# Kernel tuning notes

Hardware: AMD Instinct MI355X
Metric: run time of the kernel (lower is better)

## Reference

```python
import jax, jax.numpy as jnp
import numpy as np
from math import factorial

# irreps as (mul, l, parity): hidden = 64x0e + 32x1o + 16x2e (dim 240), edge = 1x0e + 1x1o (dim 4)
HIDDEN = [(64, 0, 1), (32, 1, -1), (16, 2, 1)]
EDGE = [(1, 0, 1), (1, 1, -1)]
N_LAYERS = 6
N_NODES = 10000
N_EDGES = 160000
N_GRAPHS = 64
IN_DIM = 3
LATENT = 128  # config.LATENT_DIM_GNN
W_STD = 0.1   # weight scale keeps 6 residual bilinear layers numerically stable

def _dim(ir):
    return sum(m * (2 * l + 1) for m, l, _ in ir)

def _slices(ir):
    out, o = [], 0
    for m, l, _ in ir:
        d = m * (2 * l + 1)
        out.append(slice(o, o + d))
        o += d
    return out

def _cg(j1, m1, j2, m2, j3, m3):
    # Condon-Shortley Clebsch-Gordan <j1 m1 j2 m2 | j3 m3> (Racah formula)
    if m1 + m2 != m3:
        return 0.0
    f = lambda n: float(factorial(n))
    pre = ((2 * j3 + 1) * f(j3 + j1 - j2) * f(j3 - j1 + j2) * f(j1 + j2 - j3) / f(j1 + j2 + j3 + 1)) ** 0.5
    pre *= (f(j3 + m3) * f(j3 - m3) * f(j1 - m1) * f(j1 + m1) * f(j2 - m2) * f(j2 + m2)) ** 0.5
    s = 0.0
    for k in range(j1 + j2 - j3 + 1):
        a = [k, j1 + j2 - j3 - k, j1 - m1 - k, j2 + m2 - k, j3 - j2 + m1 + k, j3 - j1 - m2 + k]
        if any(t < 0 for t in a):
            continue
        s += (-1) ** k / np.prod([f(t) for t in a])
    return pre * s

def _w3j_complex(l1, l2, l3):
    W = np.zeros((2 * l1 + 1, 2 * l2 + 1, 2 * l3 + 1))
    for m1 in range(-l1, l1 + 1):
        for m2 in range(-l2, l2 + 1):
            m3 = -(m1 + m2)
            if abs(m3) > l3:
                continue
            W[m1 + l1, m2 + l2, m3 + l3] = (-1) ** (l1 - l2 - m3) / np.sqrt(2 * l3 + 1) * _cg(l1, m1, l2, m2, l3, -m3)
    return W

def _A_real(l):
    # real SH in terms of complex SH: Y^r_m = sum_mu A[m, mu] Y_mu
    A = np.zeros((2 * l + 1, 2 * l + 1), dtype=complex)
    A[l, l] = 1.0
    for m in range(1, l + 1):
        A[l + m, l + m] = (-1) ** m / np.sqrt(2)
        A[l + m, l - m] = 1 / np.sqrt(2)
        A[l - m, l + m] = -1j * (-1) ** m / np.sqrt(2)
        A[l - m, l - m] = 1j / np.sqrt(2)
    return A

_W3J_CACHE = {}
def real_w3j(l1, l2, l3):
    key = (l1, l2, l3)
    if key not in _W3J_CACHE:
        T = np.einsum('ad,be,cf,def->abc', _A_real(l1), _A_real(l2), _A_real(l3), _w3j_complex(l1, l2, l3).astype(complex))
        T = np.real(T)  # exactly real when l1+l2+l3 is even (true for all paths here)
        _W3J_CACHE[key] = (T / np.linalg.norm(T)).astype(np.float32)
    return _W3J_CACHE[key]

def _paths(ir1, ir2, irout):
    ps = []
    for i1, (_, l1, p1) in enumerate(ir1):
        for i2, (_, l2, p2) in enumerate(ir2):
            for i3, (_, l3, p3) in enumerate(irout):
                if p3 == p1 * p2 and abs(l1 - l2) <= l3 <= l1 + l2:
                    ps.append((i1, i2, i3))
    return ps

MSG_PATHS = _paths(HIDDEN, EDGE, HIDDEN)
UPD_PATHS = _paths(HIDDEN, HIDDEN, HIDDEN)

def _tp_wsize(ir1, ir2, irout, paths):
    return sum(ir1[a][0] * ir2[b][0] * irout[c][0] for a, b, c in paths)

MSG_WSIZE = _tp_wsize(HIDDEN, EDGE, HIDDEN, MSG_PATHS)
UPD_WSIZE = _tp_wsize(HIDDEN, HIDDEN, HIDDEN, UPD_PATHS)
LIN_WSIZE = sum(m * m for m, _, _ in HIDDEN)

def tensor_product(x1, x2, w_flat, ir1, ir2, irout, paths):
    # FullyConnectedTensorProduct: per-path CG-coupled bilinear op with path normalization
    s1, s2, s3 = _slices(ir1), _slices(ir2), _slices(irout)
    npo = [0] * len(irout)
    for _, _, i3 in paths:
        npo[i3] += 1
    out = jnp.zeros((x1.shape[0], _dim(irout)), dtype=x1.dtype)
    off = 0
    for i1, i2, i3 in paths:
        m1, l1, _ = ir1[i1]; m2, l2, _ = ir2[i2]; m3, l3, _ = irout[i3]
        W = w_flat[off:off + m1 * m2 * m3].reshape(m1, m2, m3)
        off += m1 * m2 * m3
        C = jnp.asarray(real_w3j(l1, l2, l3), dtype=x1.dtype)
        a = x1[:, s1[i1]].reshape(-1, m1, 2 * l1 + 1)
        b = x2[:, s2[i2]].reshape(-1, m2, 2 * l2 + 1)
        alpha = 1.0 / np.sqrt(m1 * m2 * npo[i3])
        y = alpha * jnp.einsum('nui,nvj,uvw,ijk->nwk', a, b, W, C)
        out = out.at[:, s3[i3]].add(y.reshape(-1, m3 * (2 * l3 + 1)))
    return out

def irreps_linear(x, w_flat, ir):
    # e3nn Linear with identical in/out irreps: per-irrep mixing of multiplicities
    sl = _slices(ir)
    parts, off = [], 0
    for i, (m, l, _) in enumerate(ir):
        W = w_flat[off:off + m * m].reshape(m, m)
        off += m * m
        xi = x[:, sl[i]].reshape(-1, m, 2 * l + 1)
        parts.append((jnp.einsum('nui,uv->nvi', xi, W) / np.sqrt(m)).reshape(-1, m * (2 * l + 1)))
    return jnp.concatenate(parts, axis=-1)

def _forward(x, pos, w_init, w_tp_msg, w_lin_msg, w_tp_upd, w_lin_upd, w_final, edge_index, batch):
    row, col = edge_index[0], edge_index[1]
    r_vec = pos[row] - pos[col]                           # (E, 3)
    dist = jnp.linalg.norm(r_vec, axis=-1, keepdims=True)
    nvec = r_vec / jnp.maximum(dist, 1e-8)
    edge_attr = jnp.concatenate([dist, nvec], axis=-1)    # layer consumes [dist, r_vec] = 1x0e + 1x1o
    h = jnp.zeros((x.shape[0], _dim(HIDDEN)), dtype=x.dtype)
    h = h.at[:, :64].set(x @ w_init / np.sqrt(IN_DIM))    # initial Linear hits only 0e channels
    for L in range(N_LAYERS):
        hj = h[col]  # gather neighbor (source) features
        msg = tensor_product(hj, edge_attr, w_tp_msg[L], HIDDEN, EDGE, HIDDEN, MSG_PATHS) \
            + irreps_linear(hj, w_lin_msg[L], HIDDEN)
        agg = jax.ops.segment_sum(msg, row, num_segments=N_NODES)  # scatter-add aggregate
        upd = tensor_product(h, agg, w_tp_upd[L], HIDDEN, HIDDEN, HIDDEN, UPD_PATHS) \
            + irreps_linear(h, w_lin_upd[L], HIDDEN)
        h = h + upd  # residual
    scal = h[:, :64]  # 0e (invariant) channels
    cnt = jax.ops.segment_sum(jnp.ones((x.shape[0],), x.dtype), batch, num_segments=N_GRAPHS)
    pooled = jax.ops.segment_sum(scal, batch, num_segments=N_GRAPHS) / jnp.maximum(cnt, 1.0)[:, None]
    return pooled @ w_final / np.sqrt(64)

def setup_inputs() -> dict:
    key = jax.random.key(0)
    ks = jax.random.split(key, 10)
    return {
        'x': jax.random.normal(ks[0], (N_NODES, IN_DIM), jnp.float32),
        'pos': jax.random.normal(ks[1], (N_NODES, 3), jnp.float32),
        'w_init': jax.random.normal(ks[2], (IN_DIM, 64), jnp.float32),
        'w_tp_msg': jax.random.normal(ks[3], (N_LAYERS, MSG_WSIZE), jnp.float32) * W_STD,
        'w_lin_msg': jax.random.normal(ks[4], (N_LAYERS, LIN_WSIZE), jnp.float32) * W_STD,
        'w_tp_upd': jax.random.normal(ks[5], (N_LAYERS, UPD_WSIZE), jnp.float32) * W_STD,
        'w_lin_upd': jax.random.normal(ks[6], (N_LAYERS, LIN_WSIZE), jnp.float32) * W_STD,
        'w_final': jax.random.normal(ks[7], (64, LATENT), jnp.float32),
        'edge_index': jax.random.randint(ks[8], (2, N_EDGES), 0, N_NODES),
        'batch': jnp.sort(jax.random.randint(ks[9], (N_NODES,), 0, N_GRAPHS)),
    }

def reference(x, pos, w_init, w_tp_msg, w_lin_msg, w_tp_upd, w_lin_upd, w_final, edge_index, batch):
    return _forward(x, pos, w_init, w_tp_msg, w_lin_msg, w_tp_upd, w_lin_upd, w_final, edge_index, batch)
```

## Files before the change

### kernel.cpp

```cpp
#include <hip/hip_runtime.h>
#include <cmath>
#include <cstring>
#include <complex>

#define NN 10000
#define NE 160000
#define HD 240
#define ZD 912
#define NG 64
#define MSG_WS 10496
#define UPD_WS 561152
#define LIN_WS 5376

struct CMsgPre { float a000, a011, a110, a112, a211; float c101[9]; float c202[25]; };
struct CEdge   { float c011[9]; float c110[9]; float c112[45]; float c211[45]; };
struct CUpdS   { float s000; float c011[9]; float c022[25]; float c101[9]; float c202[25]; };
struct CUpdD   { float c110[9]; float c220[25]; };
struct CUpdP   { float c112[45]; float c121[45]; float c211[45]; float c222[125]; };


__global__ __launch_bounds__(256) void k_edge_attr(
    const float* __restrict__ pos, const int* __restrict__ ei, CEdge C,
    float* __restrict__ EA, float* __restrict__ CN) {
  int e = blockIdx.x * 256 + threadIdx.x;
  if (e >= NE) return;
  int r = ei[e], c = ei[NE + e];
  float dx = pos[r*3+0] - pos[c*3+0];
  float dy = pos[r*3+1] - pos[c*3+1];
  float dz = pos[r*3+2] - pos[c*3+2];
  float d = sqrtf(dx*dx + dy*dy + dz*dz);
  float inv = 1.0f / fmaxf(d, 1e-8f);
  float n0 = dx*inv, n1 = dy*inv, n2 = dz*inv;
  EA[e*4+0] = d; EA[e*4+1] = n0; EA[e*4+2] = n1; EA[e*4+3] = n2;
  float* cn = CN + (size_t)e*36;
#pragma unroll
  for (int k = 0; k < 3; k++)
    cn[k] = n0*C.c011[0*3+k] + n1*C.c011[1*3+k] + n2*C.c011[2*3+k];
#pragma unroll
  for (int i = 0; i < 3; i++)
    cn[3+i] = n0*C.c110[i*3+0] + n1*C.c110[i*3+1] + n2*C.c110[i*3+2];
#pragma unroll
  for (int i = 0; i < 3; i++)
#pragma unroll
    for (int k = 0; k < 5; k++)
      cn[6+i*5+k] = n0*C.c112[(i*3+0)*5+k] + n1*C.c112[(i*3+1)*5+k] + n2*C.c112[(i*3+2)*5+k];
#pragma unroll
  for (int i = 0; i < 5; i++)
#pragma unroll
    for (int k = 0; k < 3; k++)
      cn[21+i*3+k] = n0*C.c211[(i*3+0)*3+k] + n1*C.c211[(i*3+1)*3+k] + n2*C.c211[(i*3+2)*3+k];
}

__global__ __launch_bounds__(256) void k_h_init(
    const float* __restrict__ x, const float* __restrict__ wi, float* __restrict__ HT) {
  int n = blockIdx.x * 256 + threadIdx.x;
  int e = blockIdx.y;
  if (n >= NN) return;
  float v = 0.f;
  if (e < 64)
    v = (x[n*3+0]*wi[0*64+e] + x[n*3+1]*wi[64+e] + x[n*3+2]*wi[128+e]) * 0.57735026918962576f;
  HT[e*NN + n] = v;
}

__global__ __launch_bounds__(256) void k_node_pre(
    const float* __restrict__ HT, const float* __restrict__ Wm, const float* __restrict__ Wl,
    CMsgPre C, float* __restrict__ Z) {
  int n = blockIdx.x * 256 + threadIdx.x;
  int widx = blockIdx.y;
  if (n >= NN) return;
  float acc = 0.f;
  if (widx < 64) {
    int w = widx;
    for (int u = 0; u < 64; u++) acc += HT[u*NN+n] * Wm[u*64+w];
    acc *= C.a000;
  } else if (widx < 96) {
    int w = widx - 64;
    for (int u = 0; u < 64; u++) acc += HT[u*NN+n] * Wm[4096 + u*32+w];
    acc *= C.a011;
  } else if (widx < 192) {
    int t = widx - 96, w = t/3, k = t - w*3;
    for (int u = 0; u < 32; u++) {
      float g = HT[(64+u*3+0)*NN+n]*C.c101[0*3+k]
              + HT[(64+u*3+1)*NN+n]*C.c101[1*3+k]
              + HT[(64+u*3+2)*NN+n]*C.c101[2*3+k];
      acc += Wm[6144 + u*32+w] * g;
    }
  } else if (widx < 384) {
    int t = widx - 192, w = t/3, i = t - w*3;
    for (int u = 0; u < 32; u++) acc += HT[(64+u*3+i)*NN+n] * Wm[7168 + u*64+w];
    acc *= C.a110;
  } else if (widx < 432) {
    int t = widx - 384, w = t/3, i = t - w*3;
    for (int u = 0; u < 32; u++) acc += HT[(64+u*3+i)*NN+n] * Wm[9216 + u*16+w];
    acc *= C.a112;
  } else if (widx < 512) {
    int t = widx - 432, w = t/5, k = t - w*5;
    for (int u = 0; u < 16; u++) {
      float g = 0.f;
#pragma unroll
      for (int i = 0; i < 5; i++) g += HT[(160+u*5+i)*NN+n] * C.c202[i*5+k];
      acc += Wm[9728 + u*16+w] * g;
    }
  } else if (widx < 672) {
    int t = widx - 512, w = t/5, i = t - w*5;
    for (int u = 0; u < 16; u++) acc += HT[(160+u*5+i)*NN+n] * Wm[9984 + u*32+w];
    acc *= C.a211;
  } else {
    int e2 = widx - 672;
    if (e2 < 64) {
      for (int u = 0; u < 64; u++) acc += HT[u*NN+n] * Wl[u*64+e2];
      acc *= 0.125f;
    } else if (e2 < 160) {
      int t = e2 - 64, v = t/3, i = t - v*3;
      for (int u = 0; u < 32; u++) acc += HT[(64+u*3+i)*NN+n] * Wl[4096 + u*32+v];
      acc *= 0.17677669529663687f;
    } else {
      int t = e2 - 160, v = t/5, i = t - v*5;
      for (int u = 0; u < 16; u++) acc += HT[(160+u*5+i)*NN+n] * Wl[5120 + u*16+v];
      acc *= 0.25f;
    }
  }
  Z[(size_t)n*ZD + widx] = acc;
}

__global__ __launch_bounds__(256) void k_edge(
    const int* __restrict__ ei, const float* __restrict__ EA, const float* __restrict__ CN,
    const float* __restrict__ Z, float* __restrict__ AGG) {
  __shared__ float zsh[4][ZD];
  int lane = threadIdx.x & 63, wid = threadIdx.x >> 6;
  int wg = blockIdx.x * 4 + wid;
  int stride = gridDim.x * 4;
  int iters = (NE + stride - 1) / stride;
  for (int it = 0; it < iters; ++it) {
    int e = wg + it * stride;
    bool act = e < NE;
    int r = 0;
    float s = 0.f;
    const float* cn = CN;
    if (act) {
      r = ei[e];
      int c = ei[NE + e];
      s = EA[e*4];
      cn = CN + (size_t)e*36;
      const float* zr = Z + (size_t)c*ZD;
      for (int t = lane; t < ZD; t += 64) zsh[wid][t] = zr[t];
    }
    __syncthreads();
    if (act) {
      const float* z = zsh[wid];
#pragma unroll
      for (int j = 0; j < 4; j++) {
        int idx = lane + 64*j;
        if (idx < HD) {
          float y = z[672 + idx];
          if (idx < 64) {
            int w = idx;
            y += s * z[w];
#pragma unroll
            for (int i = 0; i < 3; i++) y += z[192 + w*3 + i] * cn[3+i];
          } else if (idx < 160) {
            int t = idx - 64, w = t/3, k = t - w*3;
            y += cn[k] * z[64 + w] + s * z[96 + t];
#pragma unroll
            for (int i = 0; i < 5; i++) y += z[512 + w*5 + i] * cn[21 + i*3 + k];
          } else {
            int t = idx - 160, w = t/5, k = t - w*5;
            y += s * z[432 + t];
#pragma unroll
            for (int i = 0; i < 3; i++) y += z[384 + w*3 + i] * cn[6 + i*5 + k];
          }
          atomicAdd(&AGG[(size_t)r*HD + idx], y);
        }
      }
    }
    __syncthreads();
  }
}

__global__ __launch_bounds__(256) void k_transpose(
    const float* __restrict__ A_nm, float* __restrict__ A_t) {
  int n = blockIdx.x * 256 + threadIdx.x;
  int e = blockIdx.y;
  if (n >= NN) return;
  A_t[e*NN + n] = A_nm[(size_t)n*HD + e];
}

__global__ __launch_bounds__(128, 2) void k_upd(
    const float* __restrict__ A,
    const float* __restrict__ B,
    const float* __restrict__ W,
    CUpdS CS, CUpdD CD, CUpdP CP,
    float* __restrict__ UPD) {
  __shared__ float4 lds4[1024];
  const int tid = threadIdx.x;
  const int n0 = blockIdx.x * 256 + tid;
  const int n1 = n0 + 128;
  const bool ok0 = n0 < NN, ok1 = n1 < NN;
  const int nc0 = ok0 ? n0 : NN - 1;
  const int nc1 = ok1 ? n1 : NN - 1;
  const int py = blockIdx.y;

#define LDA2(dst, e) { int _e=(e); dst.x = A[_e*NN+nc0]; dst.y = A[_e*NN+nc1]; }
#define LDB2(dst, e) { int _e=(e); dst.x = B[_e*NN+nc0]; dst.y = B[_e*NN+nc1]; }

  if (py < 16) {
    const int w04 = py;
    float2 y[4];
#pragma unroll
    for (int w = 0; w < 4; w++) y[w] = make_float2(0.f, 0.f);

    {
      const float4* W4 = (const float4*)W;
      for (int uc = 0; uc < 4; ++uc) {
        __syncthreads();
        for (int t = tid; t < 1024; t += 128) lds4[t] = W4[(uc*1024 + t)*16 + w04];
        __syncthreads();
        float2 ha[16];
#pragma unroll
        for (int u = 0; u < 16; ++u) {
          LDA2(ha[u], uc*16 + u);
          ha[u].x *= CS.s000; ha[u].y *= CS.s000;
        }
        for (int v = 0; v < 64; ++v) {
          float2 bv; LDB2(bv, v);
#pragma unroll
          for (int u = 0; u < 16; ++u) {
            float4 wl = lds4[u*64 + v];
            float px = ha[u].x * bv.x, qx = ha[u].y * bv.y;
            y[0].x += px*wl.x; y[0].y += qx*wl.x;
            y[1].x += px*wl.y; y[1].y += qx*wl.y;
            y[2].x += px*wl.z; y[2].y += qx*wl.z;
            y[3].x += px*wl.w; y[3].y += qx*wl.w;
          }
        }
      }
    }

    {
      const float4* W4 = (const float4*)(W + 409600);
      __syncthreads();
      for (int t = tid; t < 1024; t += 128) lds4[t] = W4[t*16 + w04];
      __syncthreads();
      for (int uc = 0; uc < 4; ++uc) {
        float2 a[8][3];
#pragma unroll
        for (int u = 0; u < 8; ++u)
#pragma unroll
          for (int i = 0; i < 3; ++i) LDA2(a[u][i], 64 + (uc*8+u)*3 + i);
        for (int v = 0; v < 32; ++v) {
          float2 b[3];
#pragma unroll
          for (int j = 0; j < 3; ++j) LDB2(b[j], 64 + v*3 + j);
          float2 bt[3];
#pragma unroll
          for (int i = 0; i < 3; ++i) {
            bt[i].x = CD.c110[i*3+0]*b[0].x + CD.c110[i*3+1]*b[1].x + CD.c110[i*3+2]*b[2].x;
            bt[i].y = CD.c110[i*3+0]*b[0].y + CD.c110[i*3+1]*b[1].y + CD.c110[i*3+2]*b[2].y;
          }
#pragma unroll
          for (int u = 0; u < 8; ++u) {
            float Dx = a[u][0].x*bt[0].x + a[u][1].x*bt[1].x + a[u][2].x*bt[2].x;
            float Dy = a[u][0].y*bt[0].y + a[u][1].y*bt[1].y + a[u][2].y*bt[2].y;
            float4 wl = lds4[(uc*8+u)*32 + v];
            y[0].x += Dx*wl.x; y[0].y += Dy*wl.x;
            y[1].x += Dx*wl.y; y[1].y += Dy*wl.y;
            y[2].x += Dx*wl.z; y[2].y += Dy*wl.z;
            y[3].x += Dx*wl.w; y[3].y += Dy*wl.w;
          }
        }
      }
    }

    {
      const float4* W4 = (const float4*)(W + 540672);
      __syncthreads();
      for (int t = tid; t < 256; t += 128) lds4[t] = W4[t*16 + w04];
      __syncthreads();
      for (int uc = 0; uc < 4; ++uc) {
        float2 a[4][5];
#pragma unroll
        for (int u = 0; u < 4; ++u)
#pragma unroll
          for (int i = 0; i < 5; ++i) LDA2(a[u][i], 160 + (uc*4+u)*5 + i);
        for (int v = 0; v < 16; ++v) {
          float2 b[5];
#pragma unroll
          for (int j = 0; j < 5; ++j) LDB2(b[j], 160 + v*5 + j);
          float2 bt[5];
#pragma unroll
          for (int i = 0; i < 5; ++i) {
            float tx = 0.f, ty = 0.f;
#pragma unroll
            for (int j = 0; j < 5; ++j) { tx += CD.c220[i*5+j]*b[j].x; ty += CD.c220[i*5+j]*b[j].y; }
            bt[i].x = tx; bt[i].y = ty;
          }
#pragma unroll
          for (int u = 0; u < 4; ++u) {
            float Dx = 0.f, Dy = 0.f;
#pragma unroll
            for (int i = 0; i < 5; ++i) { Dx += a[u][i].x*bt[i].x; Dy += a[u][i].y*bt[i].y; }
            float4 wl = lds4[(uc*4+u)*16 + v];
            y[0].x += Dx*wl.x; y[0].y += Dy*wl.x;
            y[1].x += Dx*wl.y; y[1].y += Dy*wl.y;
            y[2].x += Dx*wl.z; y[2].y += Dy*wl.z;
            y[3].x += Dx*wl.w; y[3].y += Dy*wl.w;
          }
        }
      }
    }

#pragma unroll
    for (int w = 0; w < 4; ++w) {
      if (ok0) UPD[(py*4 + w)*NN + n0] = y[w].x;
      if (ok1) UPD[(py*4 + w)*NN + n1] = y[w].y;
    }

  } else if (py < 24) {
    const int w04 = py - 16;
    float2 y[4][3];
#pragma unroll
    for (int w = 0; w < 4; w++)
#pragma unroll
      for (int k = 0; k < 3; k++) y[w][k] = make_float2(0.f, 0.f);

    {
      const float4* W4 = (const float4*)(W + 262144);
      for (int uc = 0; uc < 2; ++uc) {
        __syncthreads();
        for (int t = tid; t < 1024; t += 128) lds4[t] = W4[(uc*1024 + t)*8 + w04];
        __syncthreads();
        float2 a[32];
#pragma unroll
        for (int u = 0; u < 32; ++u) LDA2(a[u], uc*32 + u);
        for (int v = 0; v < 32; ++v) {
          float2 b[3];
#pragma unroll
          for (int j = 0; j < 3; ++j) LDB2(b[j], 64 + v*3 + j);
          float2 bc[3];
#pragma unroll
          for (int k = 0; k < 3; ++k) {
            bc[k].x = b[0].x*CS.c011[k] + b[1].x*CS.c011[3+k] + b[2].x*CS.c011[6+k];
            bc[k].y = b[0].y*CS.c011[k] + b[1].y*CS.c011[3+k] + b[2].y*CS.c011[6+k];
          }
          float2 g[4];
#pragma unroll
          for (int w = 0; w < 4; w++) g[w] = make_float2(0.f, 0.f);
#pragma unroll
          for (int u = 0; u < 32; ++u) {
            float4 wl = lds4[u*32 + v];
            g[0].x += a[u].x*wl.x; g[0].y += a[u].y*wl.x;
            g[1].x += a[u].x*wl.y; g[1].y += a[u].y*wl.y;
            g[2].x += a[u].x*wl.z; g[2].y += a[u].y*wl.z;
            g[3].x += a[u].x*wl.w; g[3].y += a[u].y*wl.w;
          }
#pragma unroll
          for (int w = 0; w < 4; ++w)
#pragma unroll
            for (int k = 0; k < 3; ++k) {
              y[w][k].x += bc[k].x*g[w].x; y[w][k].y += bc[k].y*g[w].y;
            }
        }
      }
    }

    {
      const float4* W4 = (const float4*)(W + 344064);
      for (int uc = 0; uc < 2; ++uc) {
        __syncthreads();
        for (int t = tid; t < 1024; t += 128) lds4[t] = W4[(uc*1024 + t)*8 + w04];
        __syncthreads();
        for (int vc = 0; vc < 4; ++vc) {
          float2 bv[16];
#pragma unroll
          for (int v2 = 0; v2 < 16; ++v2) LDB2(bv[v2], vc*16 + v2);
          for (int u = 0; u < 16; ++u) {
            float2 aa[3];
#pragma unroll
            for (int i = 0; i < 3; ++i) LDA2(aa[i], 64 + (uc*16+u)*3 + i);
            float2 ac[3];
#pragma unroll
            for (int k = 0; k < 3; ++k) {
              ac[k].x = aa[0].x*CS.c101[k] + aa[1].x*CS.c101[3+k] + aa[2].x*CS.c101[6+k];
              ac[k].y = aa[0].y*CS.c101[k] + aa[1].y*CS.c101[3+k] + aa[2].y*CS.c101[6+k];
            }
            float2 gp[4];
#pragma unroll
            for (int w = 0; w < 4; w++) gp[w] = make_float2(0.f, 0.f);
#pragma unroll
            for (int v2 = 0; v2 < 16; ++v2) {
              float4 wl = lds4[u*64 + vc*16 + v2];
              gp[0].x += bv[v2].x*wl.x; gp[0].y += bv[v2].y*wl.x;
              gp[1].x += bv[v2].x*wl.y; gp[1].y += bv[v2].y*wl.y;
              gp[2].x += bv[v2].x*wl.z; gp[2].y += bv[v2].y*wl.z;
              gp[3].x += bv[v2].x*wl.w; gp[3].y += bv[v2].y*wl.w;
            }
#pragma unroll
            for (int w = 0; w < 4; ++w)
#pragma unroll
              for (int k = 0; k < 3; ++k) {
                y[w][k].x += ac[k].x*gp[w].x; y[w][k].y += ac[k].y*gp[w].y;
              }
          }
        }
      }
    }

    {
      const float4* W4 = (const float4*)(W + 491520);
      __syncthreads();
      for (int t = tid; t < 512; t += 128) lds4[t] = W4[t*8 + w04];
      __syncthreads();
      for (int uc = 0; uc < 4; ++uc) {
        float2 a[8][3];
#pragma unroll
        for (int u = 0; u < 8; ++u)
#pragma unroll
          for (int i = 0; i < 3; ++i) LDA2(a[u][i], 64 + (uc*8+u)*3 + i);
        for (int v = 0; v < 16; ++v) {
          float2 b[5];
#pragma unroll
          for (int j = 0; j < 5; ++j) LDB2(b[j], 160 + v*5 + j);
          float2 bt[3][3];
#pragma unroll
          for (int i = 0; i < 3; ++i)
#pragma unroll
            for (int k = 0; k < 3; ++k) {
              float tx = 0.f, ty = 0.f;
#pragma unroll
              for (int j = 0; j < 5; ++j) { tx += b[j].x*CP.c121[(i*5+j)*3+k]; ty += b[j].y*CP.c121[(i*5+j)*3+k]; }
              bt[i][k].x = tx; bt[i][k].y = ty;
            }
#pragma unroll
          for (int u = 0; u < 8; ++u) {
            float2 P[3];
#pragma unroll
            for (int k = 0; k < 3; ++k) {
              P[k].x = a[u][0].x*bt[0][k].x + a[u][1].x*bt[1][k].x + a[u][2].x*bt[2][k].x;
              P[k].y = a[u][0].y*bt[0][k].y + a[u][1].y*bt[1][k].y + a[u][2].y*bt[2][k].y;
            }
            float4 wl = lds4[(uc*8+u)*16 + v];
#pragma unroll
            for (int k = 0; k < 3; ++k) {
              y[0][k].x += P[k].x*wl.x; y[0][k].y += P[k].y*wl.x;
              y[1][k].x += P[k].x*wl.y; y[1][k].y += P[k].y*wl.y;
              y[2][k].x += P[k].x*wl.z; y[2][k].y += P[k].y*wl.z;
              y[3][k].x += P[k].x*wl.w; y[3][k].y += P[k].y*wl.w;
            }
          }
        }
      }
    }

    {
      const float4* W4 = (const float4*)(W + 524288);
      __syncthreads();
      for (int t = tid; t < 512; t += 128) lds4[t] = W4[t*8 + w04];
      __syncthreads();
      for (int uc = 0; uc < 2; ++uc) {
        float2 a[8][5];
#pragma unroll
        for (int u = 0; u < 8; ++u)
#pragma unroll
          for (int i = 0; i < 5; ++i) LDA2(a[u][i], 160 + (uc*8+u)*5 + i);
        for (int v = 0; v < 32; ++v) {
          float2 b[3];
#pragma unroll
          for (int j = 0; j < 3; ++j) LDB2(b[j], 64 + v*3 + j);
          float2 bt[5][3];
#pragma unroll
          for (int i = 0; i < 5; ++i)
#pragma unroll
            for (int k = 0; k < 3; ++k) {
              bt[i][k].x = b[0].x*CP.c211[(i*3+0)*3+k] + b[1].x*CP.c211[(i*3+1)*3+k] + b[2].x*CP.c211[(i*3+2)*3+k];
              bt[i][k].y = b[0].y*CP.c211[(i*3+0)*3+k] + b[1].y*CP.c211[(i*3+1)*3+k] + b[2].y*CP.c211[(i*3+2)*3+k];
            }
#pragma unroll
          for (int u = 0; u < 8; ++u) {
            float2 P[3];
#pragma unroll
            for (int k = 0; k < 3; ++k) {
              float tx = 0.f, ty = 0.f;
#pragma unroll
              for (int i = 0; i < 5; ++i) { tx += a[u][i].x*bt[i][k].x; ty += a[u][i].y*bt[i][k].y; }
              P[k].x = tx; P[k].y = ty;
            }
            float4 wl = lds4[(uc*8+u)*32 + v];
#pragma unroll
            for (int k = 0; k < 3; ++k) {
              y[0][k].x += P[k].x*wl.x; y[0][k].y += P[k].y*wl.x;
              y[1][k].x += P[k].x*wl.y; y[1][k].y += P[k].y*wl.y;
              y[2][k].x += P[k].x*wl.z; y[2][k].y += P[k].y*wl.z;
              y[3][k].x += P[k].x*wl.w; y[3][k].y += P[k].y*wl.w;
            }
          }
        }
      }
    }

#pragma unroll
    for (int w = 0; w < 4; ++w)
#pragma unroll
      for (int k = 0; k < 3; ++k) {
        int e = 64 + (w04*4 + w)*3 + k;
        if (ok0) UPD[e*NN + n0] = y[w][k].x;
        if (ok1) UPD[e*NN + n1] = y[w][k].y;
      }

  } else {
    const int w04 = py - 24;
    float2 y[4][5];
#pragma unroll
    for (int w = 0; w < 4; w++)
#pragma unroll
      for (int k = 0; k < 5; k++) y[w][k] = make_float2(0.f, 0.f);

    {
      const float4* W4 = (const float4*)(W + 327680);
      __syncthreads();
      for (int t = tid; t < 1024; t += 128) lds4[t] = W4[t*4 + w04];
      __syncthreads();
      for (int uc = 0; uc < 4; ++uc) {
        float2 a[16];
#pragma unroll
        for (int u = 0; u < 16; ++u) LDA2(a[u], uc*16 + u);
        for (int v = 0; v < 16; ++v) {
          float2 b[5];
#pragma unroll
          for (int j = 0; j < 5; ++j) LDB2(b[j], 160 + v*5 + j);
          float2 bc[5];
#pragma unroll
          for (int k = 0; k < 5; ++k) {
            float tx = 0.f, ty = 0.f;
#pragma unroll
            for (int j = 0; j < 5; ++j) { tx += b[j].x*CS.c022[j*5+k]; ty += b[j].y*CS.c022[j*5+k]; }
            bc[k].x = tx; bc[k].y = ty;
          }
          float2 g[4];
#pragma unroll
          for (int w = 0; w < 4; w++) g[w] = make_float2(0.f, 0.f);
#pragma unroll
          for (int u = 0; u < 16; ++u) {
            float4 wl = lds4[(uc*16+u)*16 + v];
            g[0].x += a[u].x*wl.x; g[0].y += a[u].y*wl.x;
            g[1].x += a[u].x*wl.y; g[1].y += a[u].y*wl.y;
            g[2].x += a[u].x*wl.z; g[2].y += a[u].y*wl.z;
            g[3].x += a[u].x*wl.w; g[3].y += a[u].y*wl.w;
          }
#pragma unroll
          for (int w = 0; w < 4; ++w)
#pragma unroll
            for (int k = 0; k < 5; ++k) {
              y[w][k].x += bc[k].x*g[w].x; y[w][k].y += bc[k].y*g[w].y;
            }
        }
      }
    }

    {
      const float4* W4 = (const float4*)(W + 507904);
      __syncthreads();
      for (int t = tid; t < 1024; t += 128) lds4[t] = W4[t*4 + w04];
      __syncthreads();
      for (int vc = 0; vc < 4; ++vc) {
        float2 bv[16];
#pragma unroll
        for (int v2 = 0; v2 < 16; ++v2) LDB2(bv[v2], vc*16 + v2);
        for (int u = 0; u < 16; ++u) {
          float2 aa[5];
#pragma unroll
          for (int i = 0; i < 5; ++i) LDA2(aa[i], 160 + u*5 + i);
          float2 ac[5];
#pragma unroll
          for (int k = 0; k < 5; ++k) {
            float tx = 0.f, ty = 0.f;
#pragma unroll
            for (int i = 0; i < 5; ++i) { tx += aa[i].x*CS.c202[i*5+k]; ty += aa[i].y*CS.c202[i*5+k]; }
            ac[k].x = tx; ac[k].y = ty;
          }
          float2 gp[4];
#pragma unroll
          for (int w = 0; w < 4; w++) gp[w] = make_float2(0.f, 0.f);
#pragma unroll
          for (int v2 = 0; v2 < 16; ++v2) {
            float4 wl = lds4[u*64 + vc*16 + v2];
            gp[0].x += bv[v2].x*wl.x; gp[0].y += bv[v2].y*wl.x;
            gp[1].x += bv[v2].x*wl.y; gp[1].y += bv[v2].y*wl.y;
            gp[2].x += bv[v2].x*wl.z; gp[2].y += bv[v2].y*wl.z;
            gp[3].x += bv[v2].x*wl.w; gp[3].y += bv[v2].y*wl.w;
          }
#pragma unroll
          for (int w = 0; w < 4; ++w)
#pragma unroll
            for (int k = 0; k < 5; ++k) {
              y[w][k].x += ac[k].x*gp[w].x; y[w][k].y += ac[k].y*gp[w].y;
            }
        }
      }
    }

    {
      const float4* W4 = (const float4*)(W + 475136);
      __syncthreads();
      for (int t = tid; t < 1024; t += 128) lds4[t] = W4[t*4 + w04];
      __syncthreads();
      for (int uc = 0; uc < 4; ++uc) {
        float2 a[8][3];
#pragma unroll
        for (int u = 0; u < 8; ++u)
#pragma unroll
          for (int i = 0; i < 3; ++i) LDA2(a[u][i], 64 + (uc*8+u)*3 + i);
        for (int v = 0; v < 32; ++v) {
          float2 b[3];
#pragma unroll
          for (int j = 0; j < 3; ++j) LDB2(b[j], 64 + v*3 + j);
          float2 bt[3][5];
#pragma unroll
          for (int i = 0; i < 3; ++i)
#pragma unroll
            for (int k = 0; k < 5; ++k) {
              bt[i][k].x = b[0].x*CP.c112[(i*3+0)*5+k] + b[1].x*CP.c112[(i*3+1)*5+k] + b[2].x*CP.c112[(i*3+2)*5+k];
              bt[i][k].y = b[0].y*CP.c112[(i*3+0)*5+k] + b[1].y*CP.c112[(i*3+1)*5+k] + b[2].y*CP.c112[(i*3+2)*5+k];
            }
#pragma unroll
          for (int u = 0; u < 8; ++u) {
            float2 P[5];
#pragma unroll
            for (int k = 0; k < 5; ++k) {
              P[k].x = a[u][0].x*bt[0][k].x + a[u][1].x*bt[1][k].x + a[u][2].x*bt[2][k].x;
              P[k].y = a[u][0].y*bt[0][k].y + a[u][1].y*bt[1][k].y + a[u][2].y*bt[2][k].y;
            }
            float4 wl = lds4[(uc*8+u)*32 + v];
#pragma unroll
            for (int k = 0; k < 5; ++k) {
              y[0][k].x += P[k].x*wl.x; y[0][k].y += P[k].y*wl.x;
              y[1][k].x += P[k].x*wl.y; y[1][k].y += P[k].y*wl.y;
              y[2][k].x += P[k].x*wl.z; y[2][k].y += P[k].y*wl.z;
              y[3][k].x += P[k].x*wl.w; y[3][k].y += P[k].y*wl.w;
            }
          }
        }
      }
    }

    {
      const float4* W4 = (const float4*)(W + 557056);
      __syncthreads();
      for (int t = tid; t < 256; t += 128) lds4[t] = W4[t*4 + w04];
      __syncthreads();
      for (int v = 0; v < 16; ++v) {
        float2 b[5];
#pragma unroll
        for (int j = 0; j < 5; ++j) LDB2(b[j], 160 + v*5 + j);
        float2 bt[5][5];
#pragma unroll
        for (int i = 0; i < 5; ++i)
#pragma unroll
          for (int k = 0; k < 5; ++k) {
            float tx = 0.f, ty = 0.f;
#pragma unroll
            for (int j = 0; j < 5; ++j) { tx += b[j].x*CP.c222[(i*5+j)*5+k]; ty += b[j].y*CP.c222[(i*5+j)*5+k]; }
            bt[i][k].x = tx; bt[i][k].y = ty;
          }
        for (int u = 0; u < 16; ++u) {
          float2 aa[5];
#pragma unroll
          for (int i = 0; i < 5; ++i) LDA2(aa[i], 160 + u*5 + i);
          float2 P[5];
#pragma unroll
          for (int k = 0; k < 5; ++k) {
            float tx = 0.f, ty = 0.f;
#pragma unroll
            for (int i = 0; i < 5; ++i) { tx += aa[i].x*bt[i][k].x; ty += aa[i].y*bt[i][k].y; }
            P[k].x = tx; P[k].y = ty;
          }
          float4 wl = lds4[u*16 + v];
#pragma unroll
          for (int k = 0; k < 5; ++k) {
            y[0][k].x += P[k].x*wl.x; y[0][k].y += P[k].y*wl.x;
            y[1][k].x += P[k].x*wl.y; y[1][k].y += P[k].y*wl.y;
            y[2][k].x += P[k].x*wl.z; y[2][k].y += P[k].y*wl.z;
            y[3][k].x += P[k].x*wl.w; y[3][k].y += P[k].y*wl.w;
          }
        }
      }
    }

#pragma unroll
    for (int w = 0; w < 4; ++w)
#pragma unroll
      for (int k = 0; k < 5; ++k) {
        int e = 160 + (w04*4 + w)*5 + k;
        if (ok0) UPD[e*NN + n0] = y[w][k].x;
        if (ok1) UPD[e*NN + n1] = y[w][k].y;
      }
  }
#undef LDA2
#undef LDB2
}

__global__ __launch_bounds__(256) void k_apply(
    const float* __restrict__ Hsrc, const float* __restrict__ UPD,
    const float* __restrict__ Wl, float* __restrict__ Hdst) {
  int n = blockIdx.x * 256 + threadIdx.x;
  int e = blockIdx.y;
  if (n >= NN) return;
  float lin = 0.f;
  if (e < 64) {
    for (int u = 0; u < 64; u++) lin += Hsrc[u*NN+n] * Wl[u*64+e];
    lin *= 0.125f;
  } else if (e < 160) {
    int t = e - 64, v = t/3, i = t - v*3;
    for (int u = 0; u < 32; u++) lin += Hsrc[(64+u*3+i)*NN+n] * Wl[4096 + u*32+v];
    lin *= 0.17677669529663687f;
  } else {
    int t = e - 160, v = t/5, i = t - v*5;
    for (int u = 0; u < 16; u++) lin += Hsrc[(160+u*5+i)*NN+n] * Wl[5120 + u*16+v];
    lin *= 0.25f;
  }
  Hdst[e*NN + n] = Hsrc[e*NN + n] + UPD[e*NN + n] + lin;
}

__global__ __launch_bounds__(256) void k_cnt(const int* __restrict__ batch, float* __restrict__ CNT) {
  int n = blockIdx.x * 256 + threadIdx.x;
  if (n >= NN) return;
  atomicAdd(&CNT[batch[n]], 1.0f);
}

__global__ __launch_bounds__(256) void k_pool(
    const float* __restrict__ HT, const int* __restrict__ batch, float* __restrict__ POOL) {
  int n = blockIdx.x * 256 + threadIdx.x;
  int w = blockIdx.y;
  if (n >= NN) return;
  atomicAdd(&POOL[batch[n]*64 + w], HT[w*NN + n]);
}

__global__ __launch_bounds__(256) void k_out(
    const float* __restrict__ POOL, const float* __restrict__ CNT,
    const float* __restrict__ wf, float* __restrict__ out) {
  int tid = blockIdx.x * 256 + threadIdx.x;
  if (tid >= NG * 128) return;
  int g = tid >> 7, d = tid & 127;
  float inv = 1.0f / fmaxf(CNT[g], 1.0f);
  float acc = 0.f;
  for (int w = 0; w < 64; w++) acc += POOL[g*64 + w] * wf[w*128 + d];
  out[tid] = acc * inv * 0.125f;
}

typedef std::complex<double> cd;
static double hfact(int nn) { double f = 1; for (int i = 2; i <= nn; i++) f *= i; return f; }
static double hcg(int j1,int m1,int j2,int m2,int j3,int m3) {
  if (m1 + m2 != m3) return 0.0;
  double pre = sqrt((2*j3+1) * hfact(j3+j1-j2) * hfact(j3-j1+j2) * hfact(j1+j2-j3) / hfact(j1+j2+j3+1));
  pre *= sqrt(hfact(j3+m3)*hfact(j3-m3)*hfact(j1-m1)*hfact(j1+m1)*hfact(j2-m2)*hfact(j2+m2));
  double s = 0;
  for (int k = 0; k <= j1+j2-j3; k++) {
    int a1=j1+j2-j3-k, a2=j1-m1-k, a3=j2+m2-k, a4=j3-j2+m1+k, a5=j3-j1-m2+k;
    if (a1<0||a2<0||a3<0||a4<0||a5<0) continue;
    s += ((k&1)?-1.0:1.0) / (hfact(k)*hfact(a1)*hfact(a2)*hfact(a3)*hfact(a4)*hfact(a5));
  }
  return pre * s;
}
static void hA(int l, cd A[5][5]) {
  for (int r = 0; r < 5; r++) for (int c = 0; c < 5; c++) A[r][c] = cd(0,0);
  A[l][l] = cd(1,0);
  for (int m = 1; m <= l; m++) {
    double sg = (m & 1) ? -1.0 : 1.0;
    A[l+m][l+m] = cd(sg/sqrt(2.0), 0);
    A[l+m][l-m] = cd(1.0/sqrt(2.0), 0);
    A[l-m][l+m] = cd(0, -sg/sqrt(2.0));
    A[l-m][l-m] = cd(0, 1.0/sqrt(2.0));
  }
}
static void hw3j(int l1, int l2, int l3, double* out) {
  int n1 = 2*l1+1, n2 = 2*l2+1, n3 = 2*l3+1;
  double Wc[5][5][5]; memset(Wc, 0, sizeof Wc);
  for (int m1 = -l1; m1 <= l1; m1++) for (int m2 = -l2; m2 <= l2; m2++) {
    int m3 = -(m1+m2);
    if (m3 < -l3 || m3 > l3) continue;
    int ex = l1 - l2 - m3;
    double sg = (ex % 2 == 0) ? 1.0 : -1.0;
    Wc[m1+l1][m2+l2][m3+l3] = sg / sqrt((double)(2*l3+1)) * hcg(l1,m1,l2,m2,l3,-m3);
  }
  cd A1[5][5], A2[5][5], A3[5][5];
  hA(l1,A1); hA(l2,A2); hA(l3,A3);
  double nrm = 0;
  for (int a = 0; a < n1; a++) for (int b = 0; b < n2; b++) for (int c = 0; c < n3; c++) {
    cd acc(0,0);
    for (int d = 0; d < n1; d++) for (int e = 0; e < n2; e++) for (int f = 0; f < n3; f++) {
      double w = Wc[d][e][f];
      if (w == 0.0) continue;
      acc += A1[a][d] * A2[b][e] * A3[c][f] * w;
    }
    out[(a*n2+b)*n3+c] = acc.real();
    nrm += acc.real() * acc.real();
  }
  nrm = sqrt(nrm);
  for (int i = 0; i < n1*n2*n3; i++) out[i] /= nrm;
}

extern "C" void kernel_launch(void* const* d_in, const int* in_sizes, int n_in,
                              void* d_out, int out_size, void* d_ws, size_t ws_size,
                              hipStream_t stream) {
  const float* x        = (const float*)d_in[0];
  const float* pos      = (const float*)d_in[1];
  const float* w_init   = (const float*)d_in[2];
  const float* w_tp_msg = (const float*)d_in[3];
  const float* w_lin_msg= (const float*)d_in[4];
  const float* w_tp_upd = (const float*)d_in[5];
  const float* w_lin_upd= (const float*)d_in[6];
  const float* w_final  = (const float*)d_in[7];
  const int*   ei       = (const int*)d_in[8];
  const int*   batch    = (const int*)d_in[9];
  float* out = (float*)d_out;
  float* ws  = (float*)d_ws;

  float* EA     = ws;
  float* CN     = EA + 640000;
  float* HTA    = CN + 5760000;
  float* HTB    = HTA + 2400000;
  float* Z      = HTB + 2400000;
  float* AGG_NM = Z + 9120000;
  float* UPD_T  = AGG_NM + 2400000;
  float* AGG_T  = UPD_T + 2400000;
  float* POOL   = AGG_T + 2400000;
  float* CNT    = POOL + 4096;

  double C000d[1], C011d[9], C101d[9], C110d[9], C112d[45], C022d[25],
         C202d[25], C121d[45], C211d[45], C220d[25], C222d[125];
  hw3j(0,0,0,C000d); hw3j(0,1,1,C011d); hw3j(1,0,1,C101d); hw3j(1,1,0,C110d);
  hw3j(1,1,2,C112d); hw3j(0,2,2,C022d); hw3j(2,0,2,C202d); hw3j(1,2,1,C121d);
  hw3j(2,1,1,C211d); hw3j(2,2,0,C220d); hw3j(2,2,2,C222d);

  CMsgPre cmsg;
  cmsg.a000 = (float)(C000d[0] / sqrt(128.0));
  cmsg.a011 = (float)(1.0 / sqrt(192.0));
  cmsg.a110 = (float)(1.0 / sqrt(64.0));
  cmsg.a112 = (float)(1.0 / sqrt(64.0));
  cmsg.a211 = (float)(1.0 / sqrt(48.0));
  for (int i = 0; i < 9;  i++) cmsg.c101[i] = (float)(C101d[i] / sqrt(96.0));
  for (int i = 0; i < 25; i++) cmsg.c202[i] = (float)(C202d[i] / sqrt(32.0));

  CEdge ce;
  for (int i = 0; i < 9;  i++) ce.c011[i] = (float)C011d[i];
  for (int i = 0; i < 9;  i++) ce.c110[i] = (float)C110d[i];
  for (int i = 0; i < 45; i++) ce.c112[i] = (float)C112d[i];
  for (int i = 0; i < 45; i++) ce.c211[i] = (float)C211d[i];

  CUpdS cus;
  cus.s000 = (float)(C000d[0] / sqrt(64.0*64.0*3.0));
  for (int i = 0; i < 9;  i++) cus.c011[i] = (float)(C011d[i] / sqrt(64.0*32.0*4.0));
  for (int i = 0; i < 25; i++) cus.c022[i] = (float)(C022d[i] / sqrt(64.0*16.0*4.0));
  for (int i = 0; i < 9;  i++) cus.c101[i] = (float)(C101d[i] / sqrt(32.0*64.0*4.0));
  for (int i = 0; i < 25; i++) cus.c202[i] = (float)(C202d[i] / sqrt(16.0*64.0*4.0));

  CUpdD cud;
  for (int i = 0; i < 9;  i++) cud.c110[i] = (float)(C110d[i] / sqrt(32.0*32.0*3.0));
  for (int i = 0; i < 25; i++) cud.c220[i] = (float)(C220d[i] / sqrt(16.0*16.0*3.0));

  CUpdP cup;
  for (int i = 0; i < 45;  i++) cup.c112[i] = (float)(C112d[i] / sqrt(32.0*32.0*4.0));
  for (int i = 0; i < 45;  i++) cup.c121[i] = (float)(C121d[i] / sqrt(32.0*16.0*4.0));
  for (int i = 0; i < 45;  i++) cup.c211[i] = (float)(C211d[i] / sqrt(16.0*32.0*4.0));
  for (int i = 0; i < 125; i++) cup.c222[i] = (float)(C222d[i] / sqrt(16.0*16.0*4.0));

  k_edge_attr<<<(NE+255)/256, 256, 0, stream>>>(pos, ei, ce, EA, CN);
  k_h_init<<<dim3(40, HD), 256, 0, stream>>>(x, w_init, HTA);

  float* cur = HTA;
  float* nxt = HTB;
  for (int L = 0; L < 6; L++) {
    hipMemsetAsync(AGG_NM, 0, (size_t)2400000 * sizeof(float), stream);
    k_node_pre<<<dim3(40, ZD), 256, 0, stream>>>(cur, w_tp_msg + (size_t)L*MSG_WS,
                                                 w_lin_msg + (size_t)L*LIN_WS, cmsg, Z);
    k_edge<<<1280, 256, 0, stream>>>(ei, EA, CN, Z, AGG_NM);
    k_transpose<<<dim3(40, HD), 256, 0, stream>>>(AGG_NM, AGG_T);
    const float* Wu = w_tp_upd + (size_t)L*UPD_WS;
    k_upd<<<dim3(40, 28), 128, 0, stream>>>(cur, AGG_T, Wu, cus, cud, cup, UPD_T);
    k_apply<<<dim3(40, HD), 256, 0, stream>>>(cur, UPD_T, w_lin_upd + (size_t)L*LIN_WS, nxt);
    float* tmp = cur; cur = nxt; nxt = tmp;
  }

  hipMemsetAsync(POOL, 0, (size_t)(4096 + 64) * sizeof(float), stream);
  k_cnt<<<(NN+255)/256, 256, 0, stream>>>(batch, CNT);
  k_pool<<<dim3(40, 64), 256, 0, stream>>>(cur, batch, POOL);
  k_out<<<32, 256, 0, stream>>>(POOL, CNT, w_final, out);
}
```

Measured before the change: 5.464 ms.

## Split update tensor-product kernel into per-path pieces reduced with atomics

Each update block used to run several tensor-product paths in sequence. Now every path is its own block piece, and each piece is split four ways along one input-channel axis. Partial sums are added into the output with atomicAdd, so the grid grows from 28 to 384 pieces in y, and the launch bounds ask for 4 blocks per CU for more occupancy. The memset is widened to 4.8M floats, apparently so the atomic destination UPD_T (assumed to sit right after AGG_NM) gets zeroed. The cost is many more global atomics and repeated loads of A and B across pieces.

```diff
diff --git a/kernel.cpp b/kernel.cpp
--- a/kernel.cpp
+++ b/kernel.cpp
@@ -185,7 +185,7 @@
   A_t[e*NN + n] = A_nm[(size_t)n*HD + e];
 }
 
-__global__ __launch_bounds__(128, 2) void k_upd(
+__global__ __launch_bounds__(128, 4) void k_upd(
     const float* __restrict__ A,
     const float* __restrict__ B,
     const float* __restrict__ W,
@@ -198,482 +198,462 @@
   const bool ok0 = n0 < NN, ok1 = n1 < NN;
   const int nc0 = ok0 ? n0 : NN - 1;
   const int nc1 = ok1 ? n1 : NN - 1;
-  const int py = blockIdx.y;
+  const int piece = blockIdx.y;
+  const int rc = piece & 3;
+  const int pt = piece >> 2;
+  const float4* W4 = (const float4*)W;
 
 #define LDA2(dst, e) { int _e=(e); dst.x = A[_e*NN+nc0]; dst.y = A[_e*NN+nc1]; }
 #define LDB2(dst, e) { int _e=(e); dst.x = B[_e*NN+nc0]; dst.y = B[_e*NN+nc1]; }
-
-  if (py < 16) {
-    const int w04 = py;
+#define ATOM2(e, val) { int _e=(e); if (ok0) atomicAdd(&UPD[_e*NN+n0], val.x); if (ok1) atomicAdd(&UPD[_e*NN+n1], val.y); }
+
+  if (pt < 16) {
+    const int w04 = pt, u0 = rc << 4;
+    for (int t = tid; t < 1024; t += 128)
+      lds4[t] = W4[((u0 + (t >> 6)) * 64 + (t & 63)) * 16 + w04];
+    __syncthreads();
+    float2 ha[16];
+#pragma unroll
+    for (int u = 0; u < 16; ++u) {
+      LDA2(ha[u], u0 + u);
+      ha[u].x *= CS.s000; ha[u].y *= CS.s000;
+    }
     float2 y[4];
 #pragma unroll
     for (int w = 0; w < 4; w++) y[w] = make_float2(0.f, 0.f);
-
-    {
-      const float4* W4 = (const float4*)W;
-      for (int uc = 0; uc < 4; ++uc) {
-        __syncthreads();
-        for (int t = tid; t < 1024; t += 128) lds4[t] = W4[(uc*1024 + t)*16 + w04];
-        __syncthreads();
-        float2 ha[16];
+    for (int v = 0; v < 64; ++v) {
+      float2 bv; LDB2(bv, v);
+#pragma unroll
+      for (int u = 0; u < 16; ++u) {
+        float4 wl = lds4[u*64 + v];
+        float px = ha[u].x * bv.x, qx = ha[u].y * bv.y;
+        y[0].x += px*wl.x; y[0].y += qx*wl.x;
+        y[1].x += px*wl.y; y[1].y += qx*wl.y;
+        y[2].x += px*wl.z; y[2].y += qx*wl.z;
+        y[3].x += px*wl.w; y[3].y += qx*wl.w;
+      }
+    }
+#pragma unroll
+    for (int w = 0; w < 4; ++w) ATOM2(w04*4 + w, y[w]);
+
+  } else if (pt < 32) {
+    const int w04 = pt - 16, v0 = rc << 3;
+    for (int t = tid; t < 256; t += 128)
+      lds4[t] = W4[102400 + ((t >> 3) * 32 + v0 + (t & 7)) * 16 + w04];
+    __syncthreads();
+    float2 y[4];
+#pragma unroll
+    for (int w = 0; w < 4; w++) y[w] = make_float2(0.f, 0.f);
+    for (int uc = 0; uc < 4; ++uc) {
+      float2 a[8][3];
+#pragma unroll
+      for (int u = 0; u < 8; ++u)
+#pragma unroll
+        for (int i = 0; i < 3; ++i) LDA2(a[u][i], 64 + (uc*8+u)*3 + i);
+      for (int vl = 0; vl < 8; ++vl) {
+        float2 b[3];
+#pragma unroll
+        for (int j = 0; j < 3; ++j) LDB2(b[j], 64 + (v0+vl)*3 + j);
+        float2 bt[3];
+#pragma unroll
+        for (int i = 0; i < 3; ++i) {
+          bt[i].x = CD.c110[i*3+0]*b[0].x + CD.c110[i*3+1]*b[1].x + CD.c110[i*3+2]*b[2].x;
+          bt[i].y = CD.c110[i*3+0]*b[0].y + CD.c110[i*3+1]*b[1].y + CD.c110[i*3+2]*b[2].y;
+        }
+#pragma unroll
+        for (int u = 0; u < 8; ++u) {
+          float Dx = a[u][0].x*bt[0].x + a[u][1].x*bt[1].x + a[u][2].x*bt[2].x;
+          float Dy = a[u][0].y*bt[0].y + a[u][1].y*bt[1].y + a[u][2].y*bt[2].y;
+          float4 wl = lds4[(uc*8+u)*8 + vl];
+          y[0].x += Dx*wl.x; y[0].y += Dy*wl.x;
+          y[1].x += Dx*wl.y; y[1].y += Dy*wl.y;
+          y[2].x += Dx*wl.z; y[2].y += Dy*wl.z;
+          y[3].x += Dx*wl.w; y[3].y += Dy*wl.w;
+        }
+      }
+    }
+#pragma unroll
+    for (int w = 0; w < 4; ++w) ATOM2(w04*4 + w, y[w]);
+
+  } else if (pt < 48) {
+    const int w04 = pt - 32, v0 = rc << 2;
+    for (int t = tid; t < 64; t += 128)
+      lds4[t] = W4[135168 + ((t >> 2) * 16 + v0 + (t & 3)) * 16 + w04];
+    __syncthreads();
+    float2 y[4];
+#pragma unroll
+    for (int w = 0; w < 4; w++) y[w] = make_float2(0.f, 0.f);
+    for (int uc = 0; uc < 4; ++uc) {
+      float2 a[4][5];
+#pragma unroll
+      for (int u = 0; u < 4; ++u)
+#pragma unroll
+        for (int i = 0; i < 5; ++i) LDA2(a[u][i], 160 + (uc*4+u)*5 + i);
+      for (int vl = 0; vl < 4; ++vl) {
+        float2 b[5];
+#pragma unroll
+        for (int j = 0; j < 5; ++j) LDB2(b[j], 160 + (v0+vl)*5 + j);
+        float2 bt[5];
+#pragma unroll
+        for (int i = 0; i < 5; ++i) {
+          float tx = 0.f, ty = 0.f;
+#pragma unroll
+          for (int j = 0; j < 5; ++j) { tx += CD.c220[i*5+j]*b[j].x; ty += CD.c220[i*5+j]*b[j].y; }
+          bt[i].x = tx; bt[i].y = ty;
+        }
+#pragma unroll
+        for (int u = 0; u < 4; ++u) {
+          float Dx = 0.f, Dy = 0.f;
+#pragma unroll
+          for (int i = 0; i < 5; ++i) { Dx += a[u][i].x*bt[i].x; Dy += a[u][i].y*bt[i].y; }
+          float4 wl = lds4[(uc*4+u)*4 + vl];
+          y[0].x += Dx*wl.x; y[0].y += Dy*wl.x;
+          y[1].x += Dx*wl.y; y[1].y += Dy*wl.y;
+          y[2].x += Dx*wl.z; y[2].y += Dy*wl.z;
+          y[3].x += Dx*wl.w; y[3].y += Dy*wl.w;
+        }
+      }
+    }
+#pragma unroll
+    for (int w = 0; w < 4; ++w) ATOM2(w04*4 + w, y[w]);
+
+  } else if (pt < 56) {
+    const int w04 = pt - 48, v0 = rc << 3;
+    for (int t = tid; t < 512; t += 128)
+      lds4[t] = W4[65536 + ((t >> 3) * 32 + v0 + (t & 7)) * 8 + w04];
+    __syncthreads();
+    float2 y[4][3];
+#pragma unroll
+    for (int w = 0; w < 4; w++)
+#pragma unroll
+      for (int k = 0; k < 3; k++) y[w][k] = make_float2(0.f, 0.f);
+    for (int uc = 0; uc < 4; ++uc) {
+      float2 a[16];
+#pragma unroll
+      for (int u = 0; u < 16; ++u) LDA2(a[u], uc*16 + u);
+      for (int vl = 0; vl < 8; ++vl) {
+        float2 b[3];
+#pragma unroll
+        for (int j = 0; j < 3; ++j) LDB2(b[j], 64 + (v0+vl)*3 + j);
+        float2 bc[3];
+#pragma unroll
+        for (int k = 0; k < 3; ++k) {
+          bc[k].x = b[0].x*CS.c011[k] + b[1].x*CS.c011[3+k] + b[2].x*CS.c011[6+k];
+          bc[k].y = b[0].y*CS.c011[k] + b[1].y*CS.c011[3+k] + b[2].y*CS.c011[6+k];
+        }
+        float2 g[4];
+#pragma unroll
+        for (int w = 0; w < 4; w++) g[w] = make_float2(0.f, 0.f);
 #pragma unroll
         for (int u = 0; u < 16; ++u) {
-          LDA2(ha[u], uc*16 + u);
-          ha[u].x *= CS.s000; ha[u].y *= CS.s000;
-        }
-        for (int v = 0; v < 64; ++v) {
-          float2 bv; LDB2(bv, v);
-#pragma unroll
-          for (int u = 0; u < 16; ++u) {
-            float4 wl = lds4[u*64 + v];
-            float px = ha[u].x * bv.x, qx = ha[u].y * bv.y;
-            y[0].x += px*wl.x; y[0].y += qx*wl.x;
-            y[1].x += px*wl.y; y[1].y += qx*wl.y;
-            y[2].x += px*wl.z; y[2].y += qx*wl.z;
-            y[3].x += px*wl.w; y[3].y += qx*wl.w;
-          }
-        }
-      }
-    }
-
-    {
-      const float4* W4 = (const float4*)(W + 409600);
-      __syncthreads();
-      for (int t = tid; t < 1024; t += 128) lds4[t] = W4[t*16 + w04];
-      __syncthreads();
-      for (int uc = 0; uc < 4; ++uc) {
-        float2 a[8][3];
-#pragma unroll
-        for (int u = 0; u < 8; ++u)
-#pragma unroll
-          for (int i = 0; i < 3; ++i) LDA2(a[u][i], 64 + (uc*8+u)*3 + i);
-        for (int v = 0; v < 32; ++v) {
-          float2 b[3];
-#pragma unroll
-          for (int j = 0; j < 3; ++j) LDB2(b[j], 64 + v*3 + j);
-          float2 bt[3];
-#pragma unroll
-          for (int i = 0; i < 3; ++i) {
-            bt[i].x = CD.c110[i*3+0]*b[0].x + CD.c110[i*3+1]*b[1].x + CD.c110[i*3+2]*b[2].x;
-            bt[i].y = CD.c110[i*3+0]*b[0].y + CD.c110[i*3+1]*b[1].y + CD.c110[i*3+2]*b[2].y;
-          }
-#pragma unroll
-          for (int u = 0; u < 8; ++u) {
-            float Dx = a[u][0].x*bt[0].x + a[u][1].x*bt[1].x + a[u][2].x*bt[2].x;
-            float Dy = a[u][0].y*bt[0].y + a[u][1].y*bt[1].y + a[u][2].y*bt[2].y;
-            float4 wl = lds4[(uc*8+u)*32 + v];
-            y[0].x += Dx*wl.x; y[0].y += Dy*wl.x;
-            y[1].x += Dx*wl.y; y[1].y += Dy*wl.y;
-            y[2].x += Dx*wl.z; y[2].y += Dy*wl.z;
-            y[3].x += Dx*wl.w; y[3].y += Dy*wl.w;
-          }
-        }
-      }
-    }
-
-    {
-      const float4* W4 = (const float4*)(W + 540672);
-      __syncthreads();
-      for (int t = tid; t < 256; t += 128) lds4[t] = W4[t*16 + w04];
-      __syncthreads();
-      for (int uc = 0; uc < 4; ++uc) {
-        float2 a[4][5];
-#pragma unroll
-        for (int u = 0; u < 4; ++u)
-#pragma unroll
-          for (int i = 0; i < 5; ++i) LDA2(a[u][i], 160 + (uc*4+u)*5 + i);
-        for (int v = 0; v < 16; ++v) {
-          float2 b[5];
-#pragma unroll
-          for (int j = 0; j < 5; ++j) LDB2(b[j], 160 + v*5 + j);
-          float2 bt[5];
-#pragma unroll
-          for (int i = 0; i < 5; ++i) {
+          float4 wl = lds4[(uc*16+u)*8 + vl];
+          g[0].x += a[u].x*wl.x; g[0].y += a[u].y*wl.x;
+          g[1].x += a[u].x*wl.y; g[1].y += a[u].y*wl.y;
+          g[2].x += a[u].x*wl.z; g[2].y += a[u].y*wl.z;
+          g[3].x += a[u].x*wl.w; g[3].y += a[u].y*wl.w;
+        }
+#pragma unroll
+        for (int w = 0; w < 4; ++w)
+#pragma unroll
+          for (int k = 0; k < 3; ++k) {
+            y[w][k].x += bc[k].x*g[w].x; y[w][k].y += bc[k].y*g[w].y;
+          }
+      }
+    }
+#pragma unroll
+    for (int w = 0; w < 4; ++w)
+#pragma unroll
+      for (int k = 0; k < 3; ++k) ATOM2(64 + (w04*4 + w)*3 + k, y[w][k]);
+
+  } else if (pt < 64) {
+    const int w04 = pt - 56, v0 = rc << 4;
+    for (int t = tid; t < 512; t += 128)
+      lds4[t] = W4[86016 + ((t >> 4) * 64 + v0 + (t & 15)) * 8 + w04];
+    __syncthreads();
+    float2 y[4][3];
+#pragma unroll
+    for (int w = 0; w < 4; w++)
+#pragma unroll
+      for (int k = 0; k < 3; k++) y[w][k] = make_float2(0.f, 0.f);
+    float2 bv[16];
+#pragma unroll
+    for (int v2 = 0; v2 < 16; ++v2) LDB2(bv[v2], v0 + v2);
+    for (int u = 0; u < 32; ++u) {
+      float2 aa[3];
+#pragma unroll
+      for (int i = 0; i < 3; ++i) LDA2(aa[i], 64 + u*3 + i);
+      float2 ac[3];
+#pragma unroll
+      for (int k = 0; k < 3; ++k) {
+        ac[k].x = aa[0].x*CS.c101[k] + aa[1].x*CS.c101[3+k] + aa[2].x*CS.c101[6+k];
+        ac[k].y = aa[0].y*CS.c101[k] + aa[1].y*CS.c101[3+k] + aa[2].y*CS.c101[6+k];
+      }
+      float2 gp[4];
+#pragma unroll
+      for (int w = 0; w < 4; w++) gp[w] = make_float2(0.f, 0.f);
+#pragma unroll
+      for (int v2 = 0; v2 < 16; ++v2) {
+        float4 wl = lds4[u*16 + v2];
+        gp[0].x += bv[v2].x*wl.x; gp[0].y += bv[v2].y*wl.x;
+        gp[1].x += bv[v2].x*wl.y; gp[1].y += bv[v2].y*wl.y;
+        gp[2].x += bv[v2].x*wl.z; gp[2].y += bv[v2].y*wl.z;
+        gp[3].x += bv[v2].x*wl.w; gp[3].y += bv[v2].y*wl.w;
+      }
+#pragma unroll
+      for (int w = 0; w < 4; ++w)
+#pragma unroll
+        for (int k = 0; k < 3; ++k) {
+          y[w][k].x += ac[k].x*gp[w].x; y[w][k].y += ac[k].y*gp[w].y;
+        }
+    }
+#pragma unroll
+    for (int w = 0; w < 4; ++w)
+#pragma unroll
+      for (int k = 0; k < 3; ++k) ATOM2(64 + (w04*4 + w)*3 + k, y[w][k]);
+
+  } else if (pt < 72) {
+    const int w04 = pt - 64, v0 = rc << 2;
+    for (int t = tid; t < 128; t += 128)
+      lds4[t] = W4[122880 + ((t >> 2) * 16 + v0 + (t & 3)) * 8 + w04];
+    __syncthreads();
+    float2 y[4][3];
+#pragma unroll
+    for (int w = 0; w < 4; w++)
+#pragma unroll
+      for (int k = 0; k < 3; k++) y[w][k] = make_float2(0.f, 0.f);
+    for (int uc = 0; uc < 4; ++uc) {
+      float2 a[8][3];
+#pragma unroll
+      for (int u = 0; u < 8; ++u)
+#pragma unroll
+        for (int i = 0; i < 3; ++i) LDA2(a[u][i], 64 + (uc*8+u)*3 + i);
+      for (int vl = 0; vl < 4; ++vl) {
+        float2 b[5];
+#pragma unroll
+        for (int j = 0; j < 5; ++j) LDB2(b[j], 160 + (v0+vl)*5 + j);
+        float2 bt[3][3];
+#pragma unroll
+        for (int i = 0; i < 3; ++i)
+#pragma unroll
+          for (int k = 0; k < 3; ++k) {
             float tx = 0.f, ty = 0.f;
 #pragma unroll
-            for (int j = 0; j < 5; ++j) { tx += CD.c220[i*5+j]*b[j].x; ty += CD.c220[i*5+j]*b[j].y; }
-            bt[i].x = tx; bt[i].y = ty;
-          }
-#pragma unroll
-          for (int u = 0; u < 4; ++u) {
-            float Dx = 0.f, Dy = 0.f;
-#pragma unroll
-            for (int i = 0; i < 5; ++i) { Dx += a[u][i].x*bt[i].x; Dy += a[u][i].y*bt[i].y; }
-            float4 wl = lds4[(uc*4+u)*16 + v];
-            y[0].x += Dx*wl.x; y[0].y += Dy*wl.x;
-            y[1].x += Dx*wl.y; y[1].y += Dy*wl.y;
-            y[2].x += Dx*wl.z; y[2].y += Dy*wl.z;
-            y[3].x += Dx*wl.w; y[3].y += Dy*wl.w;
-          }
-        }
-      }
-    }
-
-#pragma unroll
-    for (int w = 0; w < 4; ++w) {
-      if (ok0) UPD[(py*4 + w)*NN + n0] = y[w].x;
-      if (ok1) UPD[(py*4 + w)*NN + n1] = y[w].y;
-    }
-
-  } else if (py < 24) {
-    const int w04 = py - 16;
+            for (int j = 0; j < 5; ++j) { tx += b[j].x*CP.c121[(i*5+j)*3+k]; ty += b[j].y*CP.c121[(i*5+j)*3+k]; }
+            bt[i][k].x = tx; bt[i][k].y = ty;
+          }
+#pragma unroll
+        for (int u = 0; u < 8; ++u) {
+          float2 P[3];
+#pragma unroll
+          for (int k = 0; k < 3; ++k) {
+            P[k].x = a[u][0].x*bt[0][k].x + a[u][1].x*bt[1][k].x + a[u][2].x*bt[2][k].x;
+            P[k].y = a[u][0].y*bt[0][k].y + a[u][1].y*bt[1][k].y + a[u][2].y*bt[2][k].y;
+          }
+          float4 wl = lds4[(uc*8+u)*4 + vl];
+#pragma unroll
+          for (int k = 0; k < 3; ++k) {
+            y[0][k].x += P[k].x*wl.x; y[0][k].y += P[k].y*wl.x;
+            y[1][k].x += P[k].x*wl.y; y[1][k].y += P[k].y*wl.y;
+            y[2][k].x += P[k].x*wl.z; y[2][k].y += P[k].y*wl.z;
+            y[3][k].x += P[k].x*wl.w; y[3][k].y += P[k].y*wl.w;
+          }
+        }
+      }
+    }
+#pragma unroll
+    for (int w = 0; w < 4; ++w)
+#pragma unroll
+      for (int k = 0; k < 3; ++k) ATOM2(64 + (w04*4 + w)*3 + k, y[w][k]);
+
+  } else if (pt < 80) {
+    const int w04 = pt - 72, v0 = rc << 3;
+    for (int t = tid; t < 128; t += 128)
+      lds4[t] = W4[131072 + ((t >> 3) * 32 + v0 + (t & 7)) * 8 + w04];
+    __syncthreads();
     float2 y[4][3];
 #pragma unroll
     for (int w = 0; w < 4; w++)
 #pragma unroll
       for (int k = 0; k < 3; k++) y[w][k] = make_float2(0.f, 0.f);
-
-    {
-      const float4* W4 = (const float4*)(W + 262144);
-      for (int uc = 0; uc < 2; ++uc) {
-        __syncthreads();
-        for (int t = tid; t < 1024; t += 128) lds4[t] = W4[(uc*1024 + t)*8 + w04];
-        __syncthreads();
-        float2 a[32];
-#pragma unroll
-        for (int u = 0; u < 32; ++u) LDA2(a[u], uc*32 + u);
-        for (int v = 0; v < 32; ++v) {
-          float2 b[3];
-#pragma unroll
-          for (int j = 0; j < 3; ++j) LDB2(b[j], 64 + v*3 + j);
-          float2 bc[3];
+    for (int uc = 0; uc < 2; ++uc) {
+      float2 a[8][5];
+#pragma unroll
+      for (int u = 0; u < 8; ++u)
+#pragma unroll
+        for (int i = 0; i < 5; ++i) LDA2(a[u][i], 160 + (uc*8+u)*5 + i);
+      for (int vl = 0; vl < 8; ++vl) {
+        float2 b[3];
+#pragma unroll
+        for (int j = 0; j < 3; ++j) LDB2(b[j], 64 + (v0+vl)*3 + j);
+        float2 bt[5][3];
+#pragma unroll
+        for (int i = 0; i < 5; ++i)
 #pragma unroll
           for (int k = 0; k < 3; ++k) {
-            bc[k].x = b[0].x*CS.c011[k] + b[1].x*CS.c011[3+k] + b[2].x*CS.c011[6+k];
-            bc[k].y = b[0].y*CS.c011[k] + b[1].y*CS.c011[3+k] + b[2].y*CS.c011[6+k];
-          }
-          float2 g[4];
-#pragma unroll
-          for (int w = 0; w < 4; w++) g[w] = make_float2(0.f, 0.f);
-#pragma unroll
-          for (int u = 0; u < 32; ++u) {
-            float4 wl = lds4[u*32 + v];
-            g[0].x += a[u].x*wl.x; g[0].y += a[u].y*wl.x;
-            g[1].x += a[u].x*wl.y; g[1].y += a[u].y*wl.y;
-            g[2].x += a[u].x*wl.z; g[2].y += a[u].y*wl.z;
-            g[3].x += a[u].x*wl.w; g[3].y += a[u].y*wl.w;
-          }
-#pragma unroll
-          for (int w = 0; w < 4; ++w)
-#pragma unroll
-            for (int k = 0; k < 3; ++k) {
-              y[w][k].x += bc[k].x*g[w].x; y[w][k].y += bc[k].y*g[w].y;
-            }
-        }
-      }
-    }
-
-    {
-      const float4* W4 = (const float4*)(W + 344064);
-      for (int uc = 0; uc < 2; ++uc) {
-        __syncthreads();
-        for (int t = tid; t < 1024; t += 128) lds4[t] = W4[(uc*1024 + t)*8 + w04];
-        __syncthreads();
-        for (int vc = 0; vc < 4; ++vc) {
-          float2 bv[16];
-#pragma unroll
-          for (int v2 = 0; v2 < 16; ++v2) LDB2(bv[v2], vc*16 + v2);
-          for (int u = 0; u < 16; ++u) {
-            float2 aa[3];
-#pragma unroll
-            for (int i = 0; i < 3; ++i) LDA2(aa[i], 64 + (uc*16+u)*3 + i);
-            float2 ac[3];
-#pragma unroll
-            for (int k = 0; k < 3; ++k) {
-              ac[k].x = aa[0].x*CS.c101[k] + aa[1].x*CS.c101[3+k] + aa[2].x*CS.c101[6+k];
-              ac[k].y = aa[0].y*CS.c101[k] + aa[1].y*CS.c101[3+k] + aa[2].y*CS.c101[6+k];
-            }
-            float2 gp[4];
-#pragma unroll
-            for (int w = 0; w < 4; w++) gp[w] = make_float2(0.f, 0.f);
-#pragma unroll
-            for (int v2 = 0; v2 < 16; ++v2) {
-              float4 wl = lds4[u*64 + vc*16 + v2];
-              gp[0].x += bv[v2].x*wl.x; gp[0].y += bv[v2].y*wl.x;
-              gp[1].x += bv[v2].x*wl.y; gp[1].y += bv[v2].y*wl.y;
-              gp[2].x += bv[v2].x*wl.z; gp[2].y += bv[v2].y*wl.z;
-              gp[3].x += bv[v2].x*wl.w; gp[3].y += bv[v2].y*wl.w;
-            }
-#pragma unroll
-            for (int w = 0; w < 4; ++w)
-#pragma unroll
-              for (int k = 0; k < 3; ++k) {
-                y[w][k].x += ac[k].x*gp[w].x; y[w][k].y += ac[k].y*gp[w].y;
-              }
-          }
-        }
-      }
-    }
-
-    {
-      const float4* W4 = (const float4*)(W + 491520);
-      __syncthreads();
-      for (int t = tid; t < 512; t += 128) lds4[t] = W4[t*8 + w04];
-      __syncthreads();
-      for (int uc = 0; uc < 4; ++uc) {
-        float2 a[8][3];
-#pragma unroll
-        for (int u = 0; u < 8; ++u)
-#pragma unroll
-          for (int i = 0; i < 3; ++i) LDA2(a[u][i], 64 + (uc*8+u)*3 + i);
-        for (int v = 0; v < 16; ++v) {
-          float2 b[5];
-#pragma unroll
-          for (int j = 0; j < 5; ++j) LDB2(b[j], 160 + v*5 + j);
-          float2 bt[3][3];
-#pragma unroll
-          for (int i = 0; i < 3; ++i)
-#pragma unroll
-            for (int k = 0; k < 3; ++k) {
-              float tx = 0.f, ty = 0.f;
-#pragma unroll
-              for (int j = 0; j < 5; ++j) { tx += b[j].x*CP.c121[(i*5+j)*3+k]; ty += b[j].y*CP.c121[(i*5+j)*3+k]; }
-              bt[i][k].x = tx; bt[i][k].y = ty;
-            }
-#pragma unroll
-          for (int u = 0; u < 8; ++u) {
-            float2 P[3];
-#pragma unroll
-            for (int k = 0; k < 3; ++k) {
-              P[k].x = a[u][0].x*bt[0][k].x + a[u][1].x*bt[1][k].x + a[u][2].x*bt[2][k].x;
-              P[k].y = a[u][0].y*bt[0][k].y + a[u][1].y*bt[1][k].y + a[u][2].y*bt[2][k].y;
-            }
-            float4 wl = lds4[(uc*8+u)*16 + v];
-#pragma unroll
-            for (int k = 0; k < 3; ++k) {
-              y[0][k].x += P[k].x*wl.x; y[0][k].y += P[k].y*wl.x;
-              y[1][k].x += P[k].x*wl.y; y[1][k].y += P[k].y*wl.y;
-              y[2][k].x += P[k].x*wl.z; y[2][k].y += P[k].y*wl.z;
-              y[3][k].x += P[k].x*wl.w; y[3][k].y += P[k].y*wl.w;
-            }
-          }
-        }
-      }
-    }
-
-    {
-      const float4* W4 = (const float4*)(W + 524288);
-      __syncthreads();
-      for (int t = tid; t < 512; t += 128) lds4[t] = W4[t*8 + w04];
-      __syncthreads();
-      for (int uc = 0; uc < 2; ++uc) {
-        float2 a[8][5];
-#pragma unroll
-        for (int u = 0; u < 8; ++u)
-#pragma unroll
-          for (int i = 0; i < 5; ++i) LDA2(a[u][i], 160 + (uc*8+u)*5 + i);
-        for (int v = 0; v < 32; ++v) {
-          float2 b[3];
-#pragma unroll
-          for (int j = 0; j < 3; ++j) LDB2(b[j], 64 + v*3 + j);
-          float2 bt[5][3];
-#pragma unroll
-          for (int i = 0; i < 5; ++i)
-#pragma unroll
-            for (int k = 0; k < 3; ++k) {
-              bt[i][k].x = b[0].x*CP.c211[(i*3+0)*3+k] + b[1].x*CP.c211[(i*3+1)*3+k] + b[2].x*CP.c211[(i*3+2)*3+k];
-              bt[i][k].y = b[0].y*CP.c211[(i*3+0)*3+k] + b[1].y*CP.c211[(i*3+1)*3+k] + b[2].y*CP.c211[(i*3+2)*3+k];
-            }
-#pragma unroll
-          for (int u = 0; u < 8; ++u) {
-            float2 P[3];
-#pragma unroll
-            for (int k = 0; k < 3; ++k) {
-              float tx = 0.f, ty = 0.f;
-#pragma unroll
-              for (int i = 0; i < 5; ++i) { tx += a[u][i].x*bt[i][k].x; ty += a[u][i].y*bt[i][k].y; }
-              P[k].x = tx; P[k].y = ty;
-            }
-            float4 wl = lds4[(uc*8+u)*32 + v];
-#pragma unroll
-            for (int k = 0; k < 3; ++k) {
-              y[0][k].x += P[k].x*wl.x; y[0][k].y += P[k].y*wl.x;
-              y[1][k].x += P[k].x*wl.y; y[1][k].y += P[k].y*wl.y;
-              y[2][k].x += P[k].x*wl.z; y[2][k].y += P[k].y*wl.z;
-              y[3][k].x += P[k].x*wl.w; y[3][k].y += P[k].y*wl.w;
-            }
-          }
-        }
-      }
-    }
-
+            bt[i][k].x = b[0].x*CP.c211[(i*3+0)*3+k] + b[1].x*CP.c211[(i*3+1)*3+k] + b[2].x*CP.c211[(i*3+2)*3+k];
+            bt[i][k].y = b[0].y*CP.c211[(i*3+0)*3+k] + b[1].y*CP.c211[(i*3+1)*3+k] + b[2].y*CP.c211[(i*3+2)*3+k];
+          }
+#pragma unroll
+        for (int u = 0; u < 8; ++u) {
+          float2 P[3];
+#pragma unroll
+          for (int k = 0; k < 3; ++k) {
+            float tx = 0.f, ty = 0.f;
+#pragma unroll
+            for (int i = 0; i < 5; ++i) { tx += a[u][i].x*bt[i][k].x; ty += a[u][i].y*bt[i][k].y; }
+            P[k].x = tx; P[k].y = ty;
+          }
+          float4 wl = lds4[(uc*8+u)*8 + vl];
+#pragma unroll
+          for (int k = 0; k < 3; ++k) {
+            y[0][k].x += P[k].x*wl.x; y[0][k].y += P[k].y*wl.x;
+            y[1][k].x += P[k].x*wl.y; y[1][k].y += P[k].y*wl.y;
+            y[2][k].x += P[k].x*wl.z; y[2][k].y += P[k].y*wl.z;
+            y[3][k].x += P[k].x*wl.w; y[3][k].y += P[k].y*wl.w;
+          }
+        }
+      }
+    }
 #pragma unroll
     for (int w = 0; w < 4; ++w)
 #pragma unroll
-      for (int k = 0; k < 3; ++k) {
-        int e = 64 + (w04*4 + w)*3 + k;
-        if (ok0) UPD[e*NN + n0] = y[w][k].x;
-        if (ok1) UPD[e*NN + n1] = y[w][k].y;
-      }
-
-  } else {
-    const int w04 = py - 24;
+      for (int k = 0; k < 3; ++k) ATOM2(64 + (w04*4 + w)*3 + k, y[w][k]);
+
+  } else if (pt < 84) {
+    const int w04 = pt - 80, v0 = rc << 2;
+    for (int t = tid; t < 256; t += 128)
+      lds4[t] = W4[81920 + ((t >> 2) * 16 + v0 + (t & 3)) * 4 + w04];
+    __syncthreads();
     float2 y[4][5];
 #pragma unroll
     for (int w = 0; w < 4; w++)
 #pragma unroll
       for (int k = 0; k < 5; k++) y[w][k] = make_float2(0.f, 0.f);
-
-    {
-      const float4* W4 = (const float4*)(W + 327680);
-      __syncthreads();
-      for (int t = tid; t < 1024; t += 128) lds4[t] = W4[t*4 + w04];
-      __syncthreads();
-      for (int uc = 0; uc < 4; ++uc) {
-        float2 a[16];
-#pragma unroll
-        for (int u = 0; u < 16; ++u) LDA2(a[u], uc*16 + u);
-        for (int v = 0; v < 16; ++v) {
-          float2 b[5];
-#pragma unroll
-          for (int j = 0; j < 5; ++j) LDB2(b[j], 160 + v*5 + j);
-          float2 bc[5];
+    for (int uc = 0; uc < 4; ++uc) {
+      float2 a[16];
+#pragma unroll
+      for (int u = 0; u < 16; ++u) LDA2(a[u], uc*16 + u);
+      for (int vl = 0; vl < 4; ++vl) {
+        float2 b[5];
+#pragma unroll
+        for (int j = 0; j < 5; ++j) LDB2(b[j], 160 + (v0+vl)*5 + j);
+        float2 bc[5];
+#pragma unroll
+        for (int k = 0; k < 5; ++k) {
+          float tx = 0.f, ty = 0.f;
+#pragma unroll
+          for (int j = 0; j < 5; ++j) { tx += b[j].x*CS.c022[j*5+k]; ty += b[j].y*CS.c022[j*5+k]; }
+          bc[k].x = tx; bc[k].y = ty;
+        }
+        float2 g[4];
+#pragma unroll
+        for (int w = 0; w < 4; w++) g[w] = make_float2(0.f, 0.f);
+#pragma unroll
+        for (int u = 0; u < 16; ++u) {
+          float4 wl = lds4[(uc*16+u)*4 + vl];
+          g[0].x += a[u].x*wl.x; g[0].y += a[u].y*wl.x;
+          g[1].x += a[u].x*wl.y; g[1].y += a[u].y*wl.y;
+          g[2].x += a[u].x*wl.z; g[2].y += a[u].y*wl.z;
+          g[3].x += a[u].x*wl.w; g[3].y += a[u].y*wl.w;
+        }
+#pragma unroll
+        for (int w = 0; w < 4; ++w)
 #pragma unroll
           for (int k = 0; k < 5; ++k) {
-            float tx = 0.f, ty = 0.f;
-#pragma unroll
-            for (int j = 0; j < 5; ++j) { tx += b[j].x*CS.c022[j*5+k]; ty += b[j].y*CS.c022[j*5+k]; }
-            bc[k].x = tx; bc[k].y = ty;
-          }
-          float2 g[4];
-#pragma unroll
-          for (int w = 0; w < 4; w++) g[w] = make_float2(0.f, 0.f);
-#pragma unroll
-          for (int u = 0; u < 16; ++u) {
-            float4 wl = lds4[(uc*16+u)*16 + v];
-            g[0].x += a[u].x*wl.x; g[0].y += a[u].y*wl.x;
-            g[1].x += a[u].x*wl.y; g[1].y += a[u].y*wl.y;
-            g[2].x += a[u].x*wl.z; g[2].y += a[u].y*wl.z;
-            g[3].x += a[u].x*wl.w; g[3].y += a[u].y*wl.w;
-          }
-#pragma unroll
-          for (int w = 0; w < 4; ++w)
-#pragma unroll
-            for (int k = 0; k < 5; ++k) {
-              y[w][k].x += bc[k].x*g[w].x; y[w][k].y += bc[k].y*g[w].y;
-            }
-        }
-      }
-    }
-
-    {
-      const float4* W4 = (const float4*)(W + 507904);
-      __syncthreads();
-      for (int t = tid; t < 1024; t += 128) lds4[t] = W4[t*4 + w04];
-      __syncthreads();
-      for (int vc = 0; vc < 4; ++vc) {
-        float2 bv[16];
-#pragma unroll
-        for (int v2 = 0; v2 < 16; ++v2) LDB2(bv[v2], vc*16 + v2);
-        for (int u = 0; u < 16; ++u) {
-          float2 aa[5];
-#pragma unroll
-          for (int i = 0; i < 5; ++i) LDA2(aa[i], 160 + u*5 + i);
-          float2 ac[5];
+            y[w][k].x += bc[k].x*g[w].x; y[w][k].y += bc[k].y*g[w].y;
+          }
+      }
+    }
+#pragma unroll
+    for (int w = 0; w < 4; ++w)
+#pragma unroll
+      for (int k = 0; k < 5; ++k) ATOM2(160 + (w04*4 + w)*5 + k, y[w][k]);
+
+  } else if (pt < 88) {
+    const int w04 = pt - 84, v0 = rc << 4;
+    for (int t = tid; t < 256; t += 128)
+      lds4[t] = W4[126976 + ((t >> 4) * 64 + v0 + (t & 15)) * 4 + w04];
+    __syncthreads();
+    float2 y[4][5];
+#pragma unroll
+    for (int w = 0; w < 4; w++)
+#pragma unroll
+      for (int k = 0; k < 5; k++) y[w][k] = make_float2(0.f, 0.f);
+    float2 bv[16];
+#pragma unroll
+    for (int v2 = 0; v2 < 16; ++v2) LDB2(bv[v2], v0 + v2);
+    for (int u = 0; u < 16; ++u) {
+      float2 aa[5];
+#pragma unroll
+      for (int i = 0; i < 5; ++i) LDA2(aa[i], 160 + u*5 + i);
+      float2 ac[5];
+#pragma unroll
+      for (int k = 0; k < 5; ++k) {
+        float tx = 0.f, ty = 0.f;
+#pragma unroll
+        for (int i = 0; i < 5; ++i) { tx += aa[i].x*CS.c202[i*5+k]; ty += aa[i].y*CS.c202[i*5+k]; }
+        ac[k].x = tx; ac[k].y = ty;
+      }
+      float2 gp[4];
+#pragma unroll
+      for (int w = 0; w < 4; w++) gp[w] = make_float2(0.f, 0.f);
+#pragma unroll
+      for (int v2 = 0; v2 < 16; ++v2) {
+        float4 wl = lds4[u*16 + v2];
+        gp[0].x += bv[v2].x*wl.x; gp[0].y += bv[v2].y*wl.x;
+        gp[1].x += bv[v2].x*wl.y; gp[1].y += bv[v2].y*wl.y;
+        gp[2].x += bv[v2].x*wl.z; gp[2].y += bv[v2].y*wl.z;
+        gp[3].x += bv[v2].x*wl.w; gp[3].y += bv[v2].y*wl.w;
+      }
+#pragma unroll
+      for (int w = 0; w < 4; ++w)
+#pragma unroll
+        for (int k = 0; k < 5; ++k) {
+          y[w][k].x += ac[k].x*gp[w].x; y[w][k].y += ac[k].y*gp[w].y;
+        }
+    }
+#pragma unroll
+    for (int w = 0; w < 4; ++w)
+#pragma unroll
+      for (int k = 0; k < 5; ++k) ATOM2(160 + (w04*4 + w)*5 + k, y[w][k]);
+
+  } else if (pt < 92) {
+    const int w04 = pt - 88, v0 = rc << 3;
+    for (int t = tid; t < 256; t += 128)
+      lds4[t] = W4[118784 + ((t >> 3) * 32 + v0 + (t & 7)) * 4 + w04];
+    __syncthreads();
+    float2 y[4][5];
+#pragma unroll
+    for (int w = 0; w < 4; w++)
+#pragma unroll
+      for (int k = 0; k < 5; k++) y[w][k] = make_float2(0.f, 0.f);
+    for (int uc = 0; uc < 4; ++uc) {
+      float2 a[8][3];
+#pragma unroll
+      for (int u = 0; u < 8; ++u)
+#pragma unroll
+        for (int i = 0; i < 3; ++i) LDA2(a[u][i], 64 + (uc*8+u)*3 + i);
+      for (int vl = 0; vl < 8; ++vl) {
+        float2 b[3];
+#pragma unroll
+        for (int j = 0; j < 3; ++j) LDB2(b[j], 64 + (v0+vl)*3 + j);
+        float2 bt[3][5];
+#pragma unroll
+        for (int i = 0; i < 3; ++i)
 #pragma unroll
           for (int k = 0; k < 5; ++k) {
-            float tx = 0.f, ty = 0.f;
-#pragma unroll
-            for (int i = 0; i < 5; ++i) { tx += aa[i].x*CS.c202[i*5+k]; ty += aa[i].y*CS.c202[i*5+k]; }
-            ac[k].x = tx; ac[k].y = ty;
-          }
-          float2 gp[4];
-#pragma unroll
-          for (int w = 0; w < 4; w++) gp[w] = make_float2(0.f, 0.f);
-#pragma unroll
-          for (int v2 = 0; v2 < 16; ++v2) {
-            float4 wl = lds4[u*64 + vc*16 + v2];
-            gp[0].x += bv[v2].x*wl.x; gp[0].y += bv[v2].y*wl.x;
-            gp[1].x += bv[v2].x*wl.y; gp[1].y += bv[v2].y*wl.y;
-            gp[2].x += bv[v2].x*wl.z; gp[2].y += bv[v2].y*wl.z;
-            gp[3].x += bv[v2].x*wl.w; gp[3].y += bv[v2].y*wl.w;
-          }
-#pragma unroll
-          for (int w = 0; w < 4; ++w)
-#pragma unroll
-            for (int k = 0; k < 5; ++k) {
-              y[w][k].x += ac[k].x*gp[w].x; y[w][k].y += ac[k].y*gp[w].y;
-            }
-        }
-      }
-    }
-
-    {
-      const float4* W4 = (const float4*)(W + 475136);
-      __syncthreads();
-      for (int t = tid; t < 1024; t += 128) lds4[t] = W4[t*4 + w04];
-      __syncthreads();
-      for (int uc = 0; uc < 4; ++uc) {
-        float2 a[8][3];
-#pragma unroll
-        for (int u = 0; u < 8; ++u)
-#pragma unroll
-          for (int i = 0; i < 3; ++i) LDA2(a[u][i], 64 + (uc*8+u)*3 + i);
-        for (int v = 0; v < 32; ++v) {
-          float2 b[3];
-#pragma unroll
-          for (int j = 0; j < 3; ++j) LDB2(b[j], 64 + v*3 + j);
-          float2 bt[3][5];
-#pragma unroll
-          for (int i = 0; i < 3; ++i)
-#pragma unroll
-            for (int k = 0; k < 5; ++k) {
-              bt[i][k].x = b[0].x*CP.c112[(i*3+0)*5+k] + b[1].x*CP.c112[(i*3+1)*5+k] + b[2].x*CP.c112[(i*3+2)*5+k];
-              bt[i][k].y = b[0].y*CP.c112[(i*3+0)*5+k] + b[1].y*CP.c112[(i*3+1)*5+k] + b[2].y*CP.c112[(i*3+2)*5+k];
-            }
-#pragma unroll
-          for (int u = 0; u < 8; ++u) {
-            float2 P[5];
-#pragma unroll
-            for (int k = 0; k < 5; ++k) {
-              P[k].x = a[u][0].x*bt[0][k].x + a[u][1].x*bt[1][k].x + a[u][2].x*bt[2][k].x;
-              P[k].y = a[u][0].y*bt[0][k].y + a[u][1].y*bt[1][k].y + a[u][2].y*bt[2][k].y;
-            }
-            float4 wl = lds4[(uc*8+u)*32 + v];
-#pragma unroll
-            for (int k = 0; k < 5; ++k) {
-              y[0][k].x += P[k].x*wl.x; y[0][k].y += P[k].y*wl.x;
-              y[1][k].x += P[k].x*wl.y; y[1][k].y += P[k].y*wl.y;
-              y[2][k].x += P[k].x*wl.z; y[2][k].y += P[k].y*wl.z;
-              y[3][k].x += P[k].x*wl.w; y[3][k].y += P[k].y*wl.w;
-            }
-          }
-        }
-      }
-    }
-
-    {
-      const float4* W4 = (const float4*)(W + 557056);
-      __syncthreads();
-      for (int t = tid; t < 256; t += 128) lds4[t] = W4[t*4 + w04];
-      __syncthreads();
-      for (int v = 0; v < 16; ++v) {
-        float2 b[5];
-#pragma unroll
-        for (int j = 0; j < 5; ++j) LDB2(b[j], 160 + v*5 + j);
-        float2 bt[5][5];
-#pragma unroll
-        for (int i = 0; i < 5; ++i)
+            bt[i][k].x = b[0].x*CP.c112[(i*3+0)*5+k] + b[1].x*CP.c112[(i*3+1)*5+k] + b[2].x*CP.c112[(i*3+2)*5+k];
+            bt[i][k].y = b[0].y*CP.c112[(i*3+0)*5+k] + b[1].y*CP.c112[(i*3+1)*5+k] + b[2].y*CP.c112[(i*3+2)*5+k];
+          }
+#pragma unroll
+        for (int u = 0; u < 8; ++u) {
+          float2 P[5];
 #pragma unroll
           for (int k = 0; k < 5; ++k) {
-            float tx = 0.f, ty = 0.f;
-#pragma unroll
-            for (int j = 0; j < 5; ++j) { tx += b[j].x*CP.c222[(i*5+j)*5+k]; ty += b[j].y*CP.c222[(i*5+j)*5+k]; }
-            bt[i][k].x = tx; bt[i][k].y = ty;
-          }
-        for (int u = 0; u < 16; ++u) {
-          float2 aa[5];
-#pragma unroll
-          for (int i = 0; i < 5; ++i) LDA2(aa[i], 160 + u*5 + i);
-          float2 P[5];
-#pragma unroll
-          for (int k = 0; k < 5; ++k) {
-            float tx = 0.f, ty = 0.f;
-#pragma unroll
-            for (int i = 0; i < 5; ++i) { tx += aa[i].x*bt[i][k].x; ty += aa[i].y*bt[i][k].y; }
-            P[k].x = tx; P[k].y = ty;
-          }
-          float4 wl = lds4[u*16 + v];
+            P[k].x = a[u][0].x*bt[0][k].x + a[u][1].x*bt[1][k].x + a[u][2].x*bt[2][k].x;
+            P[k].y = a[u][0].y*bt[0][k].y + a[u][1].y*bt[1][k].y + a[u][2].y*bt[2][k].y;
+          }
+          float4 wl = lds4[(uc*8+u)*8 + vl];
 #pragma unroll
           for (int k = 0; k < 5; ++k) {
             y[0][k].x += P[k].x*wl.x; y[0][k].y += P[k].y*wl.x;
@@ -684,18 +664,65 @@
         }
       }
     }
-
 #pragma unroll
     for (int w = 0; w < 4; ++w)
 #pragma unroll
-      for (int k = 0; k < 5; ++k) {
-        int e = 160 + (w04*4 + w)*5 + k;
-        if (ok0) UPD[e*NN + n0] = y[w][k].x;
-        if (ok1) UPD[e*NN + n1] = y[w][k].y;
-      }
+      for (int k = 0; k < 5; ++k) ATOM2(160 + (w04*4 + w)*5 + k, y[w][k]);
+
+  } else {
+    const int w04 = pt - 92, v0 = rc << 2;
+    for (int t = tid; t < 64; t += 128)
+      lds4[t] = W4[139264 + ((t >> 2) * 16 + v0 + (t & 3)) * 4 + w04];
+    __syncthreads();
+    float2 y[4][5];
+#pragma unroll
+    for (int w = 0; w < 4; w++)
+#pragma unroll
+      for (int k = 0; k < 5; k++) y[w][k] = make_float2(0.f, 0.f);
+    for (int vl = 0; vl < 4; ++vl) {
+      float2 b[5];
+#pragma unroll
+      for (int j = 0; j < 5; ++j) LDB2(b[j], 160 + (v0+vl)*5 + j);
+      float2 bt[5][5];
+#pragma unroll
+      for (int i = 0; i < 5; ++i)
+#pragma unroll
+        for (int k = 0; k < 5; ++k) {
+          float tx = 0.f, ty = 0.f;
+#pragma unroll
+          for (int j = 0; j < 5; ++j) { tx += b[j].x*CP.c222[(i*5+j)*5+k]; ty += b[j].y*CP.c222[(i*5+j)*5+k]; }
+          bt[i][k].x = tx; bt[i][k].y = ty;
+        }
+      for (int u = 0; u < 16; ++u) {
+        float2 aa[5];
+#pragma unroll
+        for (int i = 0; i < 5; ++i) LDA2(aa[i], 160 + u*5 + i);
+        float2 P[5];
+#pragma unroll
+        for (int k = 0; k < 5; ++k) {
+          float tx = 0.f, ty = 0.f;
+#pragma unroll
+          for (int i = 0; i < 5; ++i) { tx += aa[i].x*bt[i][k].x; ty += aa[i].y*bt[i][k].y; }
+          P[k].x = tx; P[k].y = ty;
+        }
+        float4 wl = lds4[u*4 + vl];
+#pragma unroll
+        for (int k = 0; k < 5; ++k) {
+          y[0][k].x += P[k].x*wl.x; y[0][k].y += P[k].y*wl.x;
+          y[1][k].x += P[k].x*wl.y; y[1][k].y += P[k].y*wl.y;
+          y[2][k].x += P[k].x*wl.z; y[2][k].y += P[k].y*wl.z;
+          y[3][k].x += P[k].x*wl.w; y[3][k].y += P[k].y*wl.w;
+        }
+      }
+    }
+#pragma unroll
+    for (int w = 0; w < 4; ++w)
+#pragma unroll
+      for (int k = 0; k < 5; ++k) ATOM2(160 + (w04*4 + w)*5 + k, y[w][k]);
   }
 #undef LDA2
 #undef LDB2
+#undef ATOM2
 }
 
 __global__ __launch_bounds__(256) void k_apply(
@@ -869,13 +896,13 @@
   float* cur = HTA;
   float* nxt = HTB;
   for (int L = 0; L < 6; L++) {
-    hipMemsetAsync(AGG_NM, 0, (size_t)2400000 * sizeof(float), stream);
+    hipMemsetAsync(AGG_NM, 0, (size_t)4800000 * sizeof(float), stream);
     k_node_pre<<<dim3(40, ZD), 256, 0, stream>>>(cur, w_tp_msg + (size_t)L*MSG_WS,
                                                  w_lin_msg + (size_t)L*LIN_WS, cmsg, Z);
     k_edge<<<1280, 256, 0, stream>>>(ei, EA, CN, Z, AGG_NM);
     k_transpose<<<dim3(40, HD), 256, 0, stream>>>(AGG_NM, AGG_T);
     const float* Wu = w_tp_upd + (size_t)L*UPD_WS;
-    k_upd<<<dim3(40, 28), 128, 0, stream>>>(cur, AGG_T, Wu, cus, cud, cup, UPD_T);
+    k_upd<<<dim3(40, 384), 128, 0, stream>>>(cur, AGG_T, Wu, cus, cud, cup, UPD_T);
     k_apply<<<dim3(40, HD), 256, 0, stream>>>(cur, UPD_T, w_lin_upd + (size_t)L*LIN_WS, nxt);
     float* tmp = cur; cur = nxt; nxt = tmp;
   }
```

Measured after the change: 4.927 ms. 1.11x faster.
